# Optimization experiments

Hardware: AMD Instinct MI355X
Metric: run time of the kernel (lower is better)

## Reference

```python
import jax, jax.numpy as jnp
import numpy as np

TEMP = 0.07
HARD_K = 512
EMB_D = 768
PROJ_D = 128
QUEUE = 32768
BATCH = 2048
NUM_CLASSES = 2


def setup_inputs() -> dict:
    key = jax.random.key(0)
    ks = jax.random.split(key, 8)
    embeddings = jax.random.normal(ks[0], (BATCH, EMB_D), dtype=jnp.float32)
    labels = jax.random.randint(ks[1], (BATCH,), 0, NUM_CLASSES)
    # projector params: Linear(D,D) -> ReLU -> Linear(D,128)
    W1 = jax.random.normal(ks[2], (EMB_D, EMB_D), dtype=jnp.float32) * 0.02
    b1 = jnp.zeros((EMB_D,), dtype=jnp.float32)
    W2 = jax.random.normal(ks[3], (EMB_D, PROJ_D), dtype=jnp.float32) * 0.02
    b2 = jnp.zeros((PROJ_D,), dtype=jnp.float32)
    # queue buffers: L2-normalized random embeddings (as in __init__) with valid labels
    qe = jax.random.normal(ks[4], (QUEUE, PROJ_D), dtype=jnp.float32)
    queue_embeddings = qe / jnp.linalg.norm(qe, axis=1, keepdims=True)
    queue_labels = jax.random.randint(ks[5], (QUEUE,), 0, NUM_CLASSES)
    return {
        'embeddings': embeddings, 'labels': labels,
        'W1': W1, 'b1': b1, 'W2': W2, 'b2': b2,
        'queue_embeddings': queue_embeddings, 'queue_labels': queue_labels,
    }


def reference(embeddings, labels, W1, b1, W2, b2, queue_embeddings, queue_labels):
    n = embeddings.shape[0]
    # projector + L2 normalize
    h = jax.nn.relu(embeddings @ W1 + b1)
    z = h @ W2 + b2
    z = z / jnp.linalg.norm(z, axis=1, keepdims=True)  # (N, 128)

    # pairwise in-batch similarities, scaled by temperature
    S = (z @ z.T) / TEMP  # (N, N)
    same = labels[:, None] == labels[None, :]
    eye = jnp.eye(n, dtype=bool)
    pos_mask = same & ~eye           # positives: same label, not self
    neg_mask = ~same                 # in-batch negatives: different label

    # logsumexp over in-batch negatives per anchor (-inf rows -> -inf, handled by logaddexp)
    neg_batch = jnp.where(neg_mask, S, -jnp.inf)
    lse_batch = jax.scipy.special.logsumexp(neg_batch, axis=1)  # (N,)

    # hard negatives from queue: opposite-label, top-K by similarity
    sims_q = z @ queue_embeddings.T  # (N, Q)
    opp = (queue_labels[None, :] != labels[:, None]) & (queue_labels[None, :] >= 0)
    masked_q = jnp.where(opp, sims_q, -jnp.inf)
    topk_vals, _ = jax.lax.top_k(masked_q, HARD_K)  # (N, K); -inf pads drop from logsumexp
    # fallback (no opposite-label entries): first K queue embeddings regardless of label
    fallback = sims_q[:, :HARD_K]
    has_opp = opp.any(axis=1, keepdims=True)
    neg_q = jnp.where(has_opp, topk_vals, fallback) / TEMP
    lse_queue = jax.scipy.special.logsumexp(neg_q, axis=1)  # (N,)

    # all negatives for anchor i: batch negatives ++ queue hard negatives
    lse_neg = jnp.logaddexp(lse_batch, lse_queue)  # (N,)

    # per positive pair (i, j): log_prob = pos_sim - logsumexp([pos_sim, negs])
    log_prob = S - jnp.logaddexp(S, lse_neg[:, None])  # (N, N)
    losses = jnp.where(pos_mask, -log_prob, 0.0)
    count = pos_mask.sum()
    return jnp.where(count > 0, losses.sum() / count.astype(losses.dtype), 0.0)
```

## Files before the change

### kernel.cpp

```cpp
#include <hip/hip_runtime.h>
#include <hip/hip_fp16.h>

#define BATCH_N   2048
#define EMB_D_    768
#define PROJ_D_   128
#define QUEUE_N   32768
#define HARD_K_   512
static constexpr float INV_T  = 1.0f / 0.07f;
static constexpr float WLO    = 0.12f;
static constexpr float S8ENC  = 255.0f / 0.88f;
static constexpr float BINW   = 0.88f / 255.0f;

typedef __attribute__((ext_vector_type(8))) short short8;
typedef __attribute__((ext_vector_type(4))) short short4v;
typedef __attribute__((ext_vector_type(4))) float f32x4;

__device__ __forceinline__ unsigned short f2bf(float f) {
    unsigned u = __float_as_uint(f);
    unsigned r = u + 0x7fffu + ((u >> 16) & 1u);
    return (unsigned short)(r >> 16);
}
__device__ __forceinline__ float bf2f(short s) {
    return __uint_as_float(((unsigned)(unsigned short)s) << 16);
}
__device__ __forceinline__ int opp_of(int mylab, const int* __restrict__ qcnt) {
    const int same = (mylab == 0) ? qcnt[0] : ((mylab == 1) ? qcnt[1] : 0);
    return qcnt[2] - same;
}

__global__ void __launch_bounds__(256) mfma_s_pack(const short* __restrict__ Ab,
                                                   const short* __restrict__ Bb,
                                                   short* __restrict__ C, int N) {
    __shared__ __align__(16) short As[128 * 128];
    __shared__ __align__(16) short Bs[128 * 128];
    const int t = threadIdx.x;
    const int lane = t & 63, wv = t >> 6;
    const int l16 = lane & 15, l4 = lane >> 4;
    const int m0 = blockIdx.y * 128, n0 = blockIdx.x * 128;

    #pragma unroll
    for (int it = 0; it < 8; ++it) {
        const int r = it * 4 + wv, row = r * 4 + l4, cg = l16 ^ (row & 15);
        __builtin_amdgcn_global_load_lds(
            (const __attribute__((address_space(1))) void*)(Ab + (size_t)(m0 + row) * 128 + cg * 8),
            (__attribute__((address_space(3))) void*)(As + r * 512), 16, 0, 0);
    }
    #pragma unroll
    for (int it = 0; it < 8; ++it) {
        const int r = it * 4 + wv, row = r * 4 + l4, cg = l16 ^ (row & 15);
        __builtin_amdgcn_global_load_lds(
            (const __attribute__((address_space(1))) void*)(Bb + (size_t)(n0 + row) * 128 + cg * 8),
            (__attribute__((address_space(3))) void*)(Bs + r * 512), 16, 0, 0);
    }
    __syncthreads();

    const int wm = (wv & 1) * 64, wn = (wv >> 1) * 64;
    f32x4 acc[4][4];
    #pragma unroll
    for (int i = 0; i < 4; ++i)
        #pragma unroll
        for (int j = 0; j < 4; ++j) acc[i][j] = f32x4{0.f, 0.f, 0.f, 0.f};

    #pragma unroll
    for (int ks = 0; ks < 4; ++ks) {
        short8 af[4], bfr[4];
        const int ch = (ks * 4 + l4) ^ l16;
        #pragma unroll
        for (int i = 0; i < 4; ++i) {
            af[i]  = *(const short8*)(As + (wm + i * 16 + l16) * 128 + ch * 8);
            bfr[i] = *(const short8*)(Bs + (wn + i * 16 + l16) * 128 + ch * 8);
        }
        #pragma unroll
        for (int i = 0; i < 4; ++i)
            #pragma unroll
            for (int j = 0; j < 4; ++j)
                acc[i][j] = __builtin_amdgcn_mfma_f32_16x16x32_bf16(af[i], bfr[j], acc[i][j], 0, 0, 0);
    }
    #pragma unroll
    for (int i = 0; i < 4; ++i)
        #pragma unroll
        for (int r = 0; r < 4; ++r) {
            const int m = m0 + wm + i * 16 + l4 * 4 + r;
            union { unsigned short u[4]; uint2 d; } pk;
            #pragma unroll
            for (int j = 0; j < 4; ++j) pk.u[j] = f2bf(acc[i][j][r]);
            *(uint2*)(C + (size_t)m * N + n0 + wn + l16 * 4) = pk.d;
        }
}

__global__ void __launch_bounds__(256) mfma_mask8(const short* __restrict__ Ab,
                                                  const short* __restrict__ Bb,
                                                  unsigned char* __restrict__ codes,
                                                  const int* __restrict__ rlabp,
                                                  const int* __restrict__ qlabp,
                                                  const int* __restrict__ colidx,
                                                  const int* __restrict__ rowmap,
                                                  const int* __restrict__ qcnt,
                                                  const int* __restrict__ rcnt) {
    const int m0 = blockIdx.y * 128;
    const int c0 = qcnt[0], c1v = qcnt[1], r0 = rcnt[0];
    int lo, hi;
    if (m0 + 128 <= r0)      { lo = c0; hi = c0 + c1v; }
    else if (m0 >= r0)       { lo = 0;  hi = c0; }
    else                     { lo = 0;  hi = c0 + c1v; }
    const int bs = blockIdx.x * 512;
    if (bs + 512 <= lo || bs >= hi) return;

    __shared__ __align__(16) short As[128 * 128];
    __shared__ __align__(16) short Bs[128 * 128];
    const int t = threadIdx.x;
    const int lane = t & 63, wv = t >> 6;
    const int l16 = lane & 15, l4 = lane >> 4;
    const int wm = (wv & 1) * 64, wn = (wv >> 1) * 64;

    #pragma unroll
    for (int it = 0; it < 8; ++it) {
        const int r = it * 4 + wv, row = r * 4 + l4, cg = l16 ^ (row & 15);
        const int srow = rowmap[m0 + row];
        __builtin_amdgcn_global_load_lds(
            (const __attribute__((address_space(1))) void*)(Ab + (size_t)srow * 128 + cg * 8),
            (__attribute__((address_space(3))) void*)(As + r * 512), 16, 0, 0);
    }
    {
        const int n0 = bs;
        #pragma unroll
        for (int it = 0; it < 8; ++it) {
            const int r = it * 4 + wv, row = r * 4 + l4, cg = l16 ^ (row & 15);
            const int scol = colidx[n0 + row];
            __builtin_amdgcn_global_load_lds(
                (const __attribute__((address_space(1))) void*)(Bb + (size_t)scol * 128 + cg * 8),
                (__attribute__((address_space(3))) void*)(Bs + r * 512), 16, 0, 0);
        }
    }

    int la[16];
    #pragma unroll
    for (int i = 0; i < 4; ++i)
        #pragma unroll
        for (int r = 0; r < 4; ++r)
            la[i * 4 + r] = rlabp[m0 + wm + i * 16 + l4 * 4 + r];
    const float C0 = 1.0f - WLO * S8ENC;
    __syncthreads();

    #pragma unroll
    for (int tt = 0; tt < 4; ++tt) {
        const int n0 = bs + tt * 128;

        f32x4 acc[4][4];
        #pragma unroll
        for (int i = 0; i < 4; ++i)
            #pragma unroll
            for (int j = 0; j < 4; ++j) acc[i][j] = f32x4{0.f, 0.f, 0.f, 0.f};

        #pragma unroll
        for (int ks = 0; ks < 4; ++ks) {
            short8 af[4], bfr[4];
            const int ch = (ks * 4 + l4) ^ l16;
            #pragma unroll
            for (int i = 0; i < 4; ++i) {
                af[i]  = *(const short8*)(As + (wm + i * 16 + l16) * 128 + ch * 8);
                bfr[i] = *(const short8*)(Bs + (wn + i * 16 + l16) * 128 + ch * 8);
            }
            #pragma unroll
            for (int i = 0; i < 4; ++i)
                #pragma unroll
                for (int j = 0; j < 4; ++j)
                    acc[i][j] = __builtin_amdgcn_mfma_f32_16x16x32_bf16(af[i], bfr[j], acc[i][j], 0, 0, 0);
        }

        if (tt < 3) {
            __syncthreads();
            const int n1 = bs + (tt + 1) * 128;
            #pragma unroll
            for (int it = 0; it < 8; ++it) {
                const int r = it * 4 + wv, row = r * 4 + l4, cg = l16 ^ (row & 15);
                const int scol = colidx[n1 + row];
                __builtin_amdgcn_global_load_lds(
                    (const __attribute__((address_space(1))) void*)(Bb + (size_t)scol * 128 + cg * 8),
                    (__attribute__((address_space(3))) void*)(Bs + r * 512), 16, 0, 0);
            }
        }

        float a0[4], a1[4];
        #pragma unroll
        for (int j = 0; j < 4; ++j) {
            const int q = qlabp[n0 + wn + j * 16 + l16];
            a0[j] = (q >= 0 && q != 0) ? C0 : -1e9f;
            a1[j] = (q >= 0 && q != 1) ? C0 : -1e9f;
        }
        #pragma unroll
        for (int i = 0; i < 4; ++i) {
            #pragma unroll
            for (int r = 0; r < 4; ++r) {
                const int m  = m0 + wm + i * 16 + l4 * 4 + r;
                const bool z = (la[i * 4 + r] == 0);
                unsigned pk = 0;
                #pragma unroll
                for (int j = 0; j < 4; ++j) {
                    const float add = z ? a0[j] : a1[j];
                    const float f = fmaf(acc[i][j][r], S8ENC, add);
#if __has_builtin(__builtin_amdgcn_cvt_pk_u8_f32)
                    pk = __builtin_amdgcn_cvt_pk_u8_f32(f, j, pk);
#else
                    const unsigned c = (unsigned)fminf(fmaxf(f, 0.0f), 255.0f);
                    pk |= c << (8 * j);
#endif
                }
                *(unsigned*)(codes + (size_t)m * QUEUE_N + n0 + wn + l16 * 4) = pk;
            }
        }
        if (tt < 3) __syncthreads();
    }
}

__global__ void __launch_bounds__(256) mfma_h64(const short* __restrict__ Ab,
                                                const short* __restrict__ Bb,
                                                const float* __restrict__ bias,
                                                short* __restrict__ C,
                                                int N, int K) {
    __shared__ __align__(16) short As[64 * 128];
    __shared__ __align__(16) short Bs[128 * 128];
    const int t = threadIdx.x;
    const int lane = t & 63, wv = t >> 6;
    const int l16 = lane & 15, l4 = lane >> 4;
    const int m0 = blockIdx.y * 64, n0 = blockIdx.x * 128;
    const int wn = wv * 32;

    f32x4 acc[4][2];
    #pragma unroll
    for (int i = 0; i < 4; ++i)
        #pragma unroll
        for (int j = 0; j < 2; ++j) acc[i][j] = f32x4{0.f, 0.f, 0.f, 0.f};

    for (int kb = 0; kb < K; kb += 128) {
        __syncthreads();
        #pragma unroll
        for (int it = 0; it < 4; ++it) {
            const int r = it * 4 + wv, row = r * 4 + l4, cg = l16 ^ (row & 15);
            __builtin_amdgcn_global_load_lds(
                (const __attribute__((address_space(1))) void*)(Ab + (size_t)(m0 + row) * K + kb + cg * 8),
                (__attribute__((address_space(3))) void*)(As + r * 512), 16, 0, 0);
        }
        #pragma unroll
        for (int it = 0; it < 8; ++it) {
            const int r = it * 4 + wv, row = r * 4 + l4, cg = l16 ^ (row & 15);
            __builtin_amdgcn_global_load_lds(
                (const __attribute__((address_space(1))) void*)(Bb + (size_t)(n0 + row) * K + kb + cg * 8),
                (__attribute__((address_space(3))) void*)(Bs + r * 512), 16, 0, 0);
        }
        __syncthreads();
        #pragma unroll
        for (int ks = 0; ks < 4; ++ks) {
            short8 af[4], bfr[2];
            const int ch = (ks * 4 + l4) ^ l16;
            #pragma unroll
            for (int i = 0; i < 4; ++i)
                af[i] = *(const short8*)(As + (i * 16 + l16) * 128 + ch * 8);
            #pragma unroll
            for (int j = 0; j < 2; ++j)
                bfr[j] = *(const short8*)(Bs + (wn + j * 16 + l16) * 128 + ch * 8);
            #pragma unroll
            for (int i = 0; i < 4; ++i)
                #pragma unroll
                for (int j = 0; j < 2; ++j)
                    acc[i][j] = __builtin_amdgcn_mfma_f32_16x16x32_bf16(af[i], bfr[j], acc[i][j], 0, 0, 0);
        }
    }

    float bsv[2];
    #pragma unroll
    for (int j = 0; j < 2; ++j) bsv[j] = bias[n0 + wn + j * 16 + l16];
    #pragma unroll
    for (int i = 0; i < 4; ++i)
        #pragma unroll
        for (int r = 0; r < 4; ++r) {
            const int m = m0 + i * 16 + l4 * 4 + r;
            #pragma unroll
            for (int j = 0; j < 2; ++j) {
                const int n = n0 + wn + j * 16 + l16;
                const float v = fmaxf(acc[i][j][r] + bsv[j], 0.0f);
                C[(size_t)m * N + n] = (short)f2bf(v);
            }
        }
}

__global__ void __launch_bounds__(256) mfma_z_norm64(const short* __restrict__ Ab,
                                                     const short* __restrict__ Bb,
                                                     const float* __restrict__ bias,
                                                     short* __restrict__ zb) {
    __shared__ __align__(16) short As[64 * 128];
    __shared__ __align__(16) short Bs[128 * 128];
    __shared__ float ssq[64];
    const int t = threadIdx.x;
    const int lane = t & 63, wv = t >> 6;
    const int l16 = lane & 15, l4 = lane >> 4;
    const int m0 = blockIdx.x * 64;
    const int wn = wv * 32;
    const int K = EMB_D_;

    if (t < 64) ssq[t] = 0.0f;

    f32x4 acc[4][2];
    #pragma unroll
    for (int i = 0; i < 4; ++i)
        #pragma unroll
        for (int j = 0; j < 2; ++j) acc[i][j] = f32x4{0.f, 0.f, 0.f, 0.f};

    for (int kb = 0; kb < K; kb += 128) {
        __syncthreads();
        #pragma unroll
        for (int it = 0; it < 4; ++it) {
            const int r = it * 4 + wv, row = r * 4 + l4, cg = l16 ^ (row & 15);
            __builtin_amdgcn_global_load_lds(
                (const __attribute__((address_space(1))) void*)(Ab + (size_t)(m0 + row) * K + kb + cg * 8),
                (__attribute__((address_space(3))) void*)(As + r * 512), 16, 0, 0);
        }
        #pragma unroll
        for (int it = 0; it < 8; ++it) {
            const int r = it * 4 + wv, row = r * 4 + l4, cg = l16 ^ (row & 15);
            __builtin_amdgcn_global_load_lds(
                (const __attribute__((address_space(1))) void*)(Bb + (size_t)(row) * K + kb + cg * 8),
                (__attribute__((address_space(3))) void*)(Bs + r * 512), 16, 0, 0);
        }
        __syncthreads();
        #pragma unroll
        for (int ks = 0; ks < 4; ++ks) {
            short8 af[4], bfr[2];
            const int ch = (ks * 4 + l4) ^ l16;
            #pragma unroll
            for (int i = 0; i < 4; ++i)
                af[i] = *(const short8*)(As + (i * 16 + l16) * 128 + ch * 8);
            #pragma unroll
            for (int j = 0; j < 2; ++j)
                bfr[j] = *(const short8*)(Bs + (wn + j * 16 + l16) * 128 + ch * 8);
            #pragma unroll
            for (int i = 0; i < 4; ++i)
                #pragma unroll
                for (int j = 0; j < 2; ++j)
                    acc[i][j] = __builtin_amdgcn_mfma_f32_16x16x32_bf16(af[i], bfr[j], acc[i][j], 0, 0, 0);
        }
    }

    float bsv[2];
    #pragma unroll
    for (int j = 0; j < 2; ++j) bsv[j] = bias[wn + j * 16 + l16];
    #pragma unroll
    for (int i = 0; i < 4; ++i)
        #pragma unroll
        for (int r = 0; r < 4; ++r) {
            float p = 0.0f;
            #pragma unroll
            for (int j = 0; j < 2; ++j) {
                acc[i][j][r] += bsv[j];
                p += acc[i][j][r] * acc[i][j][r];
            }
            #pragma unroll
            for (int o = 8; o > 0; o >>= 1) p += __shfl_xor(p, o);
            if (l16 == 0) atomicAdd(&ssq[i * 16 + l4 * 4 + r], p);
        }
    __syncthreads();
    #pragma unroll
    for (int i = 0; i < 4; ++i)
        #pragma unroll
        for (int r = 0; r < 4; ++r) {
            const int lrow = i * 16 + l4 * 4 + r;
            const float inv = rsqrtf(ssq[lrow]);
            #pragma unroll
            for (int j = 0; j < 2; ++j)
                zb[(size_t)(m0 + lrow) * PROJ_D_ + wn + j * 16 + l16] =
                    (short)f2bf(acc[i][j][r] * inv);
        }
}

__global__ void __launch_bounds__(256) prep(const float* __restrict__ emb, short* __restrict__ embb,
                                            const float* __restrict__ queue, short* __restrict__ qb,
                                            const int* __restrict__ qlab, int* __restrict__ qcnt,
                                            const float* __restrict__ W1, short* __restrict__ w1t,
                                            const float* __restrict__ W2, short* __restrict__ w2t,
                                            const int* __restrict__ labels, int* __restrict__ rcnt) {
    __shared__ float tile[64][65];
    const int b = blockIdx.x, t = threadIdx.x;
    if (b < 1536) {
        const int i = b * 256 + t;
        const float4 f = ((const float4*)emb)[i];
        short4v o = {(short)f2bf(f.x), (short)f2bf(f.y), (short)f2bf(f.z), (short)f2bf(f.w)};
        ((short4v*)embb)[i] = o;
    } else if (b < 5632) {
        const int i = (b - 1536) * 256 + t;
        const float4 f = ((const float4*)queue)[i];
        short4v o = {(short)f2bf(f.x), (short)f2bf(f.y), (short)f2bf(f.z), (short)f2bf(f.w)};
        ((short4v*)qb)[i] = o;
    } else if (b < 5664) {
        const int i = (b - 5632) * 256 + t;
        int c0 = 0, c1 = 0, cv = 0;
        for (int j = i; j < QUEUE_N; j += 8192) {
            const int q = qlab[j];
            c0 += (q == 0); c1 += (q == 1); cv += (q >= 0);
        }
        #pragma unroll
        for (int o = 32; o > 0; o >>= 1) {
            c0 += __shfl_xor(c0, o); c1 += __shfl_xor(c1, o); cv += __shfl_xor(cv, o);
        }
        if ((t & 63) == 0) {
            atomicAdd(&qcnt[0], c0); atomicAdd(&qcnt[1], c1); atomicAdd(&qcnt[2], cv);
        }
    } else if (b < 5832) {
        const int bid = b - 5664;
        const float* A; short* At; int R, C, bx, by;
        if (bid < 144) { A = W1; At = w1t; R = EMB_D_; C = EMB_D_;  bx = (bid % 12) * 64; by = (bid / 12) * 64; }
        else { const int b2 = bid - 144; A = W2; At = w2t; R = EMB_D_; C = PROJ_D_; bx = (b2 & 1) * 64; by = (b2 >> 1) * 64; }
        const int tc = t & 63, tg = t >> 6;
        #pragma unroll
        for (int i = 0; i < 16; i++) {
            const int r = tg * 16 + i;
            tile[r][tc] = A[(size_t)(by + r) * C + bx + tc];
        }
        __syncthreads();
        #pragma unroll
        for (int i = 0; i < 16; i++) {
            const int r = tg * 16 + i;
            At[(size_t)(bx + r) * R + by + tc] = (short)f2bf(tile[tc][r]);
        }
    } else {
        int c = 0;
        for (int j = t; j < BATCH_N; j += 256) c += (labels[j] == 0);
        #pragma unroll
        for (int o = 32; o > 0; o >>= 1) c += __shfl_xor(c, o);
        if ((t & 63) == 0) atomicAdd(&rcnt[0], c);
    }
}

__global__ void __launch_bounds__(256) build_perm(const int* __restrict__ qlab,
                                                  const int* __restrict__ labels,
                                                  const int* __restrict__ qcnt,
                                                  const int* __restrict__ rcnt,
                                                  int* __restrict__ colidx,
                                                  int* __restrict__ qlabp,
                                                  int* __restrict__ rowmap,
                                                  int* __restrict__ rlabp,
                                                  int* __restrict__ pc) {
    const int t = threadIdx.x, lane = t & 63, wv = t >> 6;
    __shared__ int wcnt[4][3];
    __shared__ int gbase[3];
    const unsigned long long below = (1ull << lane) - 1ull;
    if (blockIdx.x < 128) {
        const int j = blockIdx.x * 256 + t;
        const int q = qlab[j];
        const int cls = (q == 0) ? 0 : ((q == 1) ? 1 : 2);
        const unsigned long long b0 = __ballot(cls == 0);
        const unsigned long long b1 = __ballot(cls == 1);
        const unsigned long long b2 = __ballot(cls == 2);
        const int rank = (cls == 0) ? __popcll(b0 & below)
                       : ((cls == 1) ? __popcll(b1 & below) : __popcll(b2 & below));
        if (lane == 0) {
            wcnt[wv][0] = __popcll(b0); wcnt[wv][1] = __popcll(b1); wcnt[wv][2] = __popcll(b2);
        }
        __syncthreads();
        if (t < 3) {
            const int tot = wcnt[0][t] + wcnt[1][t] + wcnt[2][t] + wcnt[3][t];
            gbase[t] = atomicAdd(&pc[t], tot);
        }
        __syncthreads();
        int wb = 0;
        #pragma unroll
        for (int w = 0; w < 4; ++w) if (w < wv) wb += wcnt[w][cls];
        const int cbase = (cls == 0) ? 0 : ((cls == 1) ? qcnt[0] : qcnt[0] + qcnt[1]);
        const int pos = cbase + gbase[cls] + wb + rank;
        colidx[pos] = j; qlabp[pos] = q;
    } else {
        const int r = (blockIdx.x - 128) * 256 + t;
        const int l = labels[r];
        const int cls = (l == 0) ? 0 : 1;
        const unsigned long long b0 = __ballot(cls == 0);
        const unsigned long long b1 = __ballot(cls == 1);
        const int rank = (cls == 0) ? __popcll(b0 & below) : __popcll(b1 & below);
        if (lane == 0) { wcnt[wv][0] = __popcll(b0); wcnt[wv][1] = __popcll(b1); }
        __syncthreads();
        if (t < 2) {
            const int tot = wcnt[0][t] + wcnt[1][t] + wcnt[2][t] + wcnt[3][t];
            gbase[t] = atomicAdd(&pc[3 + t], tot);
        }
        __syncthreads();
        int wb = 0;
        #pragma unroll
        for (int w = 0; w < 4; ++w) if (w < wv) wb += wcnt[w][cls];
        const int cbase = (cls == 0) ? 0 : rcnt[0];
        const int pos = cbase + gbase[cls] + wb + rank;
        rowmap[pos] = r; rlabp[pos] = l;
    }
}

__global__ void __launch_bounds__(256) topk_lse_u8(const unsigned char* __restrict__ codes,
                                                   const int* __restrict__ qcnt,
                                                   const int* __restrict__ rlabp,
                                                   const int* __restrict__ rowmap,
                                                   float* __restrict__ lseq,
                                                   int* __restrict__ flag) {
    const int p = blockIdx.x, t = threadIdx.x;
    const int orig  = rowmap[p];
    const int myLab = rlabp[p];
    const int opp   = opp_of(myLab, qcnt);
    if (opp < HARD_K_) {
        if (t == 0) flag[orig] = 0;
        return;
    }
    __shared__ int hist[256];
    __shared__ int suf[256];
    __shared__ int s_bin;
    __shared__ float scf[4];
    hist[t] = 0;
    __syncthreads();

    const int c0 = qcnt[0];
    const int lo = (myLab == 0) ? c0 : 0;
    const int hi = (myLab == 0) ? c0 + qcnt[1] : c0;
    const int klo = (lo & ~511) >> 4;
    const int khi = ((hi + 511) & ~511) >> 4;

    const uint4* rowp = (const uint4*)(codes + (size_t)p * QUEUE_N);
    for (int k = klo + t; k < khi; k += 256) {
        const uint4 u = rowp[k];
        const unsigned w[4] = {u.x, u.y, u.z, u.w};
        #pragma unroll
        for (int q = 0; q < 4; q++)
            #pragma unroll
            for (int s = 0; s < 4; s++) {
                const int c = (w[q] >> (8 * s)) & 0xFF;
                if (c) atomicAdd(&hist[c], 1);
            }
    }
    __syncthreads();

    suf[t] = hist[t];
    __syncthreads();
    for (int off = 1; off < 256; off <<= 1) {
        int add = (t + off < 256) ? suf[t + off] : 0;
        __syncthreads();
        suf[t] += add;
        __syncthreads();
    }
    const int total = suf[1];
    if (total < HARD_K_) {
        if (t == 0) flag[orig] = 0;
        return;
    }
    {
        const int above = (t < 255) ? suf[t + 1] : 0;
        if (suf[t] >= HARD_K_ && above < HARD_K_) s_bin = t;
    }
    __syncthreads();
    const int b = s_bin;

    float e = 0.0f;
    if (t > b && hist[t]) e = (float)hist[t] * __expf((WLO + ((float)t - 0.5f) * BINW - 1.0f) * INV_T);
    #pragma unroll
    for (int o = 32; o > 0; o >>= 1) e += __shfl_xor(e, o);
    if ((t & 63) == 0) scf[t >> 6] = e;
    __syncthreads();
    if (t == 0) {
        const float Eab  = scf[0] + scf[1] + scf[2] + scf[3];
        const int   cab  = (b < 255) ? suf[b + 1] : 0;
        const float ebin = __expf((WLO + ((float)b - 0.5f) * BINW - 1.0f) * INV_T);
        const float sadj = Eab + (float)(HARD_K_ - cab) * ebin;
        lseq[orig] = INV_T + __logf(sadj);
        flag[orig] = 1;
    }
}

__device__ __forceinline__ void find_crossing(int* hist, int* grp, int target,
                                              int* s_bin, int* s_chi) {
    const int t = threadIdx.x;
    const int b0 = hist[4*t], b1 = hist[4*t+1], b2 = hist[4*t+2], b3 = hist[4*t+3];
    grp[t] = b0 + b1 + b2 + b3;
    __syncthreads();
    for (int off = 1; off < 256; off <<= 1) {
        int add = (t + off < 256) ? grp[t + off] : 0;
        __syncthreads();
        grp[t] += add;
        __syncthreads();
    }
    int cab = (t < 255) ? grp[t + 1] : 0;
    const int hb[4] = {b0, b1, b2, b3};
    #pragma unroll
    for (int i = 3; i >= 0; i--) {
        const int h = hb[i];
        if (cab < target && cab + h >= target) { *s_bin = 4*t + i; *s_chi = cab; }
        cab += h;
    }
    __syncthreads();
}

#define FOR_ALL_VALS(BODY)                                                   \
    _Pragma("unroll")                                                        \
    for (int _k = 0; _k < 64; _k++) {                                        \
        const float2 _f = __half22float2(*(const __half2*)&dv[_k]);          \
        { const float v = _f.x; BODY }                                       \
        { const float v = _f.y; BODY }                                       \
    }

__global__ void __launch_bounds__(256) topk_lse_fallback(const short* __restrict__ zb,
                                                         const short* __restrict__ qb,
                                                         const int* __restrict__ labels,
                                                         const int* __restrict__ qlab,
                                                         const int* __restrict__ qcnt,
                                                         const int* __restrict__ flag,
                                                         float* __restrict__ lseq) {
    const int row = blockIdx.x, t = threadIdx.x;
    if (flag[row]) return;
    const int opp = opp_of(labels[row], qcnt);

    __shared__ float zrow[128];
    __shared__ int hist[1024];
    __shared__ int grp[256];
    __shared__ int s_bin, s_chi, s_bin2, s_chi2;
    __shared__ float scf[4]; __shared__ int sci[4];
    if (t < 128) zrow[t] = bf2f(zb[(size_t)row * 128 + t]);
    __syncthreads();

    const int mylab = labels[row];
    unsigned dv[64];
    float rm = -1e30f, rs = 0.0f;
    for (int k = 0; k < 128; k++) {
        const int j = t + 256 * k;
        float d = 0.0f;
        #pragma unroll
        for (int c = 0; c < 16; ++c) {
            const short8 qv = *(const short8*)(qb + (size_t)j * 128 + c * 8);
            #pragma unroll
            for (int e = 0; e < 8; ++e) d += zrow[c * 8 + e] * bf2f(qv[e]);
        }
        if (j < HARD_K_) {
            const float sv = d * INV_T;
            if (sv > rm) { rs = rs * __expf(rm - sv) + 1.0f; rm = sv; }
            else         { rs += __expf(sv - rm); }
        }
        const int q = qlab[j];
        const float mv = (q != mylab && q >= 0) ? d : -65504.0f;
        const __half h = __float2half(mv);
        unsigned short* p = (unsigned short*)&dv[k >> 1];
        p[k & 1] = *(const unsigned short*)&h;
    }

    if (opp == 0) {
        #pragma unroll
        for (int o = 32; o > 0; o >>= 1) {
            const float om = __shfl_xor(rm, o), os = __shfl_xor(rs, o);
            const float nm = fmaxf(rm, om);
            rs = rs * __expf(rm - nm) + os * __expf(om - nm);
            rm = nm;
        }
        if ((t & 63) == 0) { scf[t >> 6] = rm; ((float*)sci)[t >> 6] = rs; }
        __syncthreads();
        if (t == 0) {
            float M = -1e30f, Sx = 0.0f;
            for (int w = 0; w < 4; w++) {
                const float nm = fmaxf(M, scf[w]);
                Sx = Sx * __expf(M - nm) + ((float*)sci)[w] * __expf(scf[w] - nm);
                M = nm;
            }
            lseq[row] = M + __logf(Sx);
        }
        return;
    }
    if (opp < HARD_K_) {
        float mm = -1e30f, ss = 0.0f;
        FOR_ALL_VALS(
            if (v > -60000.0f) {
                const float sv = v * INV_T;
                if (sv > mm) { ss = ss * __expf(mm - sv) + 1.0f; mm = sv; }
                else         { ss += __expf(sv - mm); }
            } )
        #pragma unroll
        for (int o = 32; o > 0; o >>= 1) {
            const float om = __shfl_xor(mm, o), os = __shfl_xor(ss, o);
            const float nm = fmaxf(mm, om);
            ss = ss * __expf(mm - nm) + os * __expf(om - nm);
            mm = nm;
        }
        if ((t & 63) == 0) { scf[t >> 6] = mm; ((float*)sci)[t >> 6] = ss; }
        __syncthreads();
        if (t == 0) {
            float M = -1e30f, Sx = 0.0f;
            for (int w = 0; w < 4; w++) {
                const float nm = fmaxf(M, scf[w]);
                Sx = Sx * __expf(M - nm) + ((float*)sci)[w] * __expf(scf[w] - nm);
                M = nm;
            }
            lseq[row] = M + __logf(Sx);
        }
        return;
    }

    float mloc = -1e30f;
    FOR_ALL_VALS( mloc = fmaxf(mloc, v); )
    #pragma unroll
    for (int o = 32; o > 0; o >>= 1) mloc = fmaxf(mloc, __shfl_xor(mloc, o));
    if ((t & 63) == 0) scf[t >> 6] = mloc;
    __syncthreads();
    const float m = fmaxf(fmaxf(scf[0], scf[1]), fmaxf(scf[2], scf[3]));

    int c1 = 0, c2 = 0;
    const float w1 = m - 0.25f, w2 = m - 1.0f;
    FOR_ALL_VALS( c1 += (v >= w1); c2 += (v >= w2); )
    #pragma unroll
    for (int o = 32; o > 0; o >>= 1) { c1 += __shfl_xor(c1, o); c2 += __shfl_xor(c2, o); }
    if ((t & 63) == 0) { sci[t >> 6] = c1; }
    __syncthreads();
    const int C1 = sci[0] + sci[1] + sci[2] + sci[3];
    __syncthreads();
    if ((t & 63) == 0) { sci[t >> 6] = c2; }
    __syncthreads();
    const int C2 = sci[0] + sci[1] + sci[2] + sci[3];

    float lo;
    if      (C1 >= HARD_K_) lo = w1;
    else if (C2 >= HARD_K_) lo = w2;
    else                    lo = -1.01f;
    const float range = m - lo;
    const float scale = 1024.0f / range;

    for (int k = t; k < 1024; k += 256) hist[k] = 0;
    __syncthreads();
    FOR_ALL_VALS(
        if (v >= lo) {
            const float bf = fminf((v - lo) * scale, 1023.0f);
            atomicAdd(&hist[(int)bf], 1);
        } )
    __syncthreads();
    find_crossing(hist, grp, HARD_K_, &s_bin, &s_chi);
    const int   bin1 = s_bin, chi1 = s_chi;
    const float binw = range * (1.0f / 1024.0f);
    const float lo1  = lo + bin1 * binw;
    const float ssc  = 1024.0f / binw;

    for (int k = t; k < 1024; k += 256) hist[k] = 0;
    __syncthreads();
    FOR_ALL_VALS(
        if (v >= lo) {
            const float bf = fminf((v - lo) * scale, 1023.0f);
            if ((int)bf == bin1) {
                const float sf = fminf(fmaxf((v - lo1) * ssc, 0.0f), 1023.0f);
                atomicAdd(&hist[(int)sf], 1);
            }
        } )
    __syncthreads();
    find_crossing(hist, grp, HARD_K_ - chi1, &s_bin2, &s_chi2);
    const float thr = lo1 + s_bin2 * (binw * (1.0f / 1024.0f));

    float sl = 0.0f; int cg = 0;
    FOR_ALL_VALS( if (v > thr) { cg++; sl += __expf((v - m) * INV_T); } )
    #pragma unroll
    for (int o = 32; o > 0; o >>= 1) { sl += __shfl_xor(sl, o); cg += __shfl_xor(cg, o); }
    if ((t & 63) == 0) { scf[t >> 6] = sl; sci[t >> 6] = cg; }
    __syncthreads();
    if (t == 0) {
        const float slt = scf[0] + scf[1] + scf[2] + scf[3];
        const int   cgt = sci[0] + sci[1] + sci[2] + sci[3];
        const float sadj = slt + ((float)HARD_K_ - (float)cgt) * __expf((thr - m) * INV_T);
        lseq[row] = m * INV_T + __logf(sadj);
    }
}

__global__ void __launch_bounds__(256) batch_row_loss(const short* __restrict__ S,
                                                      const int* __restrict__ labels,
                                                      const float* __restrict__ lse_queue,
                                                      float* __restrict__ part_out,
                                                      int* __restrict__ cnt_out) {
    const int t = threadIdx.x;
    const int wv = t >> 6, lane = t & 63;
    const int row = blockIdx.x * 4 + wv;
    __shared__ int plab[BATCH_N];
    for (int idx = t; idx < BATCH_N; idx += 256) {
        const int col = (idx & ~63) + ((idx & 3) << 4) + ((idx >> 2) & 15);
        plab[idx] = labels[col];
    }
    __syncthreads();
    const int myLab = labels[row];
    const uint4* rp = (const uint4*)(S + (size_t)row * BATCH_N);

    float v[32]; int lb[32];
    #pragma unroll
    for (int kk = 0; kk < 4; kk++) {
        const uint4 u = rp[lane + 64 * kk];
        const unsigned w[4] = {u.x, u.y, u.z, u.w};
        const int base = (lane + 64 * kk) * 8;
        #pragma unroll
        for (int q = 0; q < 4; q++) {
            v[kk * 8 + 2 * q]     = __uint_as_float(w[q] << 16);
            v[kk * 8 + 2 * q + 1] = __uint_as_float(w[q] & 0xFFFF0000u);
            lb[kk * 8 + 2 * q]     = plab[base + 2 * q];
            lb[kk * 8 + 2 * q + 1] = plab[base + 2 * q + 1];
        }
    }

    const float REF = INV_T;
    float sneg = 0.0f;
    #pragma unroll
    for (int k = 0; k < 32; k++) {
        const float ev = __expf(v[k] * INV_T - REF);
        sneg += (lb[k] != myLab) ? ev : 0.0f;
    }
    #pragma unroll
    for (int o = 32; o > 0; o >>= 1) sneg += __shfl_xor(sneg, o);
    const float lseb = (sneg > 0.0f) ? REF + __logf(sneg) : -1e30f;
    const float Lq = lse_queue[row];
    const float mx0 = fmaxf(lseb, Lq), mn0 = fminf(lseb, Lq);
    const float L = mx0 + __logf(1.0f + __expf(mn0 - mx0));

    float part = 0.0f; int cnt = 0;
    #pragma unroll
    for (int k = 0; k < 32; k++) {
        const int idx = ((lane + 64 * (k >> 3)) * 8) + (k & 7);
        const int col = (idx & ~63) + ((idx & 3) << 4) + ((idx >> 2) & 15);
        if (lb[k] == myLab && col != row) {
            const float sv = v[k] * INV_T;
            const float mx = fmaxf(sv, L), mn = fminf(sv, L);
            part += (mx - sv) + __logf(1.0f + __expf(mn - mx));
            cnt++;
        }
    }
    #pragma unroll
    for (int o = 32; o > 0; o >>= 1) { part += __shfl_xor(part, o); cnt += __shfl_xor(cnt, o); }
    if (lane == 0) { part_out[row] = part; cnt_out[row] = cnt; }
}

__global__ void __launch_bounds__(256) finalize_loss(const float* __restrict__ part,
                                                     const int* __restrict__ cnt,
                                                     float* __restrict__ out) {
    const int t = threadIdx.x;
    float s = 0.0f; int c = 0;
    #pragma unroll
    for (int k = 0; k < 8; k++) { s += part[t + 256 * k]; c += cnt[t + 256 * k]; }
    #pragma unroll
    for (int o = 32; o > 0; o >>= 1) { s += __shfl_xor(s, o); c += __shfl_xor(c, o); }
    __shared__ float sf[4]; __shared__ int sc[4];
    if ((t & 63) == 0) { sf[t >> 6] = s; sc[t >> 6] = c; }
    __syncthreads();
    if (t == 0) {
        const float st = sf[0] + sf[1] + sf[2] + sf[3];
        const int   ct = sc[0] + sc[1] + sc[2] + sc[3];
        out[0] = (ct > 0) ? (st / (float)ct) : 0.0f;
    }
}

extern "C" void kernel_launch(void* const* d_in, const int* in_sizes, int n_in,
                              void* d_out, int out_size, void* d_ws, size_t ws_size,
                              hipStream_t stream) {
    const float* emb    = (const float*)d_in[0];
    const int*   labels = (const int*)  d_in[1];
    const float* W1     = (const float*)d_in[2];
    const float* b1     = (const float*)d_in[3];
    const float* W2     = (const float*)d_in[4];
    const float* b2     = (const float*)d_in[5];
    const float* queue  = (const float*)d_in[6];
    const int*   qlab   = (const int*)  d_in[7];

    char* ws = (char*)d_ws;
    short*         Sbuf  = (short*)        (ws);
    unsigned char* codes = (unsigned char*)(ws + 16777216);
    short*         embb  = (short*)        (ws + 83886080);
    short*         hbf   = (short*)        (ws + 87031808);
    short*         zb    = (short*)        (ws + 90177536);
    short*         qb    = (short*)        (ws + 90701824);
    short*         w1t   = (short*)        (ws + 99090432);
    short*         w2t   = (short*)        (ws + 100270080);
    float*         lseq  = (float*)        (ws + 100466688);
    int*           flag  = (int*)          (ws + 100474880);
    int*           qcnt  = (int*)          (ws + 100483072);
    float*         partb = (float*)        (ws + 100483136);
    int*           cntb  = (int*)          (ws + 100491328);
    int*           rcnt  = (int*)          (ws + 100499520);
    int*           pc    = (int*)          (ws + 100499584);
    int*           colidx= (int*)          (ws + 100499648);
    int*           qlabp = (int*)          (ws + 100630720);
    int*           rowmap= (int*)          (ws + 100761792);
    int*           rlabp = (int*)          (ws + 100769984);

    hipMemsetAsync(ws + 100474880, 0, 24768, stream);

    dim3 blk(256);
    prep<<<dim3(5833), blk, 0, stream>>>(emb, embb, queue, qb, qlab, qcnt, W1, w1t, W2, w2t, labels, rcnt);
    build_perm<<<dim3(136), blk, 0, stream>>>(qlab, labels, qcnt, rcnt, colidx, qlabp, rowmap, rlabp, pc);
    mfma_h64<<<dim3(EMB_D_ / 128, BATCH_N / 64), blk, 0, stream>>>(embb, w1t, b1, hbf, EMB_D_, EMB_D_);
    mfma_z_norm64<<<dim3(BATCH_N / 64), blk, 0, stream>>>(hbf, w2t, b2, zb);
    mfma_mask8<<<dim3(QUEUE_N / 512, BATCH_N / 128), blk, 0, stream>>>(zb, qb, codes, rlabp, qlabp, colidx, rowmap, qcnt, rcnt);
    topk_lse_u8<<<BATCH_N, blk, 0, stream>>>(codes, qcnt, rlabp, rowmap, lseq, flag);
    topk_lse_fallback<<<BATCH_N, blk, 0, stream>>>(zb, qb, labels, qlab, qcnt, flag, lseq);
    mfma_s_pack<<<dim3(BATCH_N / 128, BATCH_N / 128), blk, 0, stream>>>(zb, zb, Sbuf, BATCH_N);
    batch_row_loss<<<BATCH_N / 4, blk, 0, stream>>>(Sbuf, labels, lseq, partb, cntb);
    finalize_loss<<<1, blk, 0, stream>>>(partb, cntb, (float*)d_out);
}
```

Measured before the change: 166.4 us.

## Fuse launches: merge perm build into z-norm, and topk, fallback, S-GEMM into one kernel

Result: slower. 192.6 us (+15.7%).

```diff
diff --git a/kernel.cpp b/kernel.cpp
--- a/kernel.cpp
+++ b/kernel.cpp
@@ -28,356 +28,13 @@
     return qcnt[2] - same;
 }
 
-__global__ void __launch_bounds__(256) mfma_s_pack(const short* __restrict__ Ab,
-                                                   const short* __restrict__ Bb,
-                                                   short* __restrict__ C, int N) {
-    __shared__ __align__(16) short As[128 * 128];
-    __shared__ __align__(16) short Bs[128 * 128];
-    const int t = threadIdx.x;
-    const int lane = t & 63, wv = t >> 6;
-    const int l16 = lane & 15, l4 = lane >> 4;
-    const int m0 = blockIdx.y * 128, n0 = blockIdx.x * 128;
-
-    #pragma unroll
-    for (int it = 0; it < 8; ++it) {
-        const int r = it * 4 + wv, row = r * 4 + l4, cg = l16 ^ (row & 15);
-        __builtin_amdgcn_global_load_lds(
-            (const __attribute__((address_space(1))) void*)(Ab + (size_t)(m0 + row) * 128 + cg * 8),
-            (__attribute__((address_space(3))) void*)(As + r * 512), 16, 0, 0);
-    }
-    #pragma unroll
-    for (int it = 0; it < 8; ++it) {
-        const int r = it * 4 + wv, row = r * 4 + l4, cg = l16 ^ (row & 15);
-        __builtin_amdgcn_global_load_lds(
-            (const __attribute__((address_space(1))) void*)(Bb + (size_t)(n0 + row) * 128 + cg * 8),
-            (__attribute__((address_space(3))) void*)(Bs + r * 512), 16, 0, 0);
-    }
-    __syncthreads();
-
-    const int wm = (wv & 1) * 64, wn = (wv >> 1) * 64;
-    f32x4 acc[4][4];
-    #pragma unroll
-    for (int i = 0; i < 4; ++i)
-        #pragma unroll
-        for (int j = 0; j < 4; ++j) acc[i][j] = f32x4{0.f, 0.f, 0.f, 0.f};
-
-    #pragma unroll
-    for (int ks = 0; ks < 4; ++ks) {
-        short8 af[4], bfr[4];
-        const int ch = (ks * 4 + l4) ^ l16;
-        #pragma unroll
-        for (int i = 0; i < 4; ++i) {
-            af[i]  = *(const short8*)(As + (wm + i * 16 + l16) * 128 + ch * 8);
-            bfr[i] = *(const short8*)(Bs + (wn + i * 16 + l16) * 128 + ch * 8);
-        }
-        #pragma unroll
-        for (int i = 0; i < 4; ++i)
-            #pragma unroll
-            for (int j = 0; j < 4; ++j)
-                acc[i][j] = __builtin_amdgcn_mfma_f32_16x16x32_bf16(af[i], bfr[j], acc[i][j], 0, 0, 0);
-    }
-    #pragma unroll
-    for (int i = 0; i < 4; ++i)
-        #pragma unroll
-        for (int r = 0; r < 4; ++r) {
-            const int m = m0 + wm + i * 16 + l4 * 4 + r;
-            union { unsigned short u[4]; uint2 d; } pk;
-            #pragma unroll
-            for (int j = 0; j < 4; ++j) pk.u[j] = f2bf(acc[i][j][r]);
-            *(uint2*)(C + (size_t)m * N + n0 + wn + l16 * 4) = pk.d;
-        }
-}
-
-__global__ void __launch_bounds__(256) mfma_mask8(const short* __restrict__ Ab,
-                                                  const short* __restrict__ Bb,
-                                                  unsigned char* __restrict__ codes,
-                                                  const int* __restrict__ rlabp,
-                                                  const int* __restrict__ qlabp,
-                                                  const int* __restrict__ colidx,
-                                                  const int* __restrict__ rowmap,
-                                                  const int* __restrict__ qcnt,
-                                                  const int* __restrict__ rcnt) {
-    const int m0 = blockIdx.y * 128;
-    const int c0 = qcnt[0], c1v = qcnt[1], r0 = rcnt[0];
-    int lo, hi;
-    if (m0 + 128 <= r0)      { lo = c0; hi = c0 + c1v; }
-    else if (m0 >= r0)       { lo = 0;  hi = c0; }
-    else                     { lo = 0;  hi = c0 + c1v; }
-    const int bs = blockIdx.x * 512;
-    if (bs + 512 <= lo || bs >= hi) return;
-
-    __shared__ __align__(16) short As[128 * 128];
-    __shared__ __align__(16) short Bs[128 * 128];
-    const int t = threadIdx.x;
-    const int lane = t & 63, wv = t >> 6;
-    const int l16 = lane & 15, l4 = lane >> 4;
-    const int wm = (wv & 1) * 64, wn = (wv >> 1) * 64;
-
-    #pragma unroll
-    for (int it = 0; it < 8; ++it) {
-        const int r = it * 4 + wv, row = r * 4 + l4, cg = l16 ^ (row & 15);
-        const int srow = rowmap[m0 + row];
-        __builtin_amdgcn_global_load_lds(
-            (const __attribute__((address_space(1))) void*)(Ab + (size_t)srow * 128 + cg * 8),
-            (__attribute__((address_space(3))) void*)(As + r * 512), 16, 0, 0);
-    }
-    {
-        const int n0 = bs;
-        #pragma unroll
-        for (int it = 0; it < 8; ++it) {
-            const int r = it * 4 + wv, row = r * 4 + l4, cg = l16 ^ (row & 15);
-            const int scol = colidx[n0 + row];
-            __builtin_amdgcn_global_load_lds(
-                (const __attribute__((address_space(1))) void*)(Bb + (size_t)scol * 128 + cg * 8),
-                (__attribute__((address_space(3))) void*)(Bs + r * 512), 16, 0, 0);
-        }
-    }
-
-    int la[16];
-    #pragma unroll
-    for (int i = 0; i < 4; ++i)
-        #pragma unroll
-        for (int r = 0; r < 4; ++r)
-            la[i * 4 + r] = rlabp[m0 + wm + i * 16 + l4 * 4 + r];
-    const float C0 = 1.0f - WLO * S8ENC;
-    __syncthreads();
-
-    #pragma unroll
-    for (int tt = 0; tt < 4; ++tt) {
-        const int n0 = bs + tt * 128;
-
-        f32x4 acc[4][4];
-        #pragma unroll
-        for (int i = 0; i < 4; ++i)
-            #pragma unroll
-            for (int j = 0; j < 4; ++j) acc[i][j] = f32x4{0.f, 0.f, 0.f, 0.f};
-
-        #pragma unroll
-        for (int ks = 0; ks < 4; ++ks) {
-            short8 af[4], bfr[4];
-            const int ch = (ks * 4 + l4) ^ l16;
-            #pragma unroll
-            for (int i = 0; i < 4; ++i) {
-                af[i]  = *(const short8*)(As + (wm + i * 16 + l16) * 128 + ch * 8);
-                bfr[i] = *(const short8*)(Bs + (wn + i * 16 + l16) * 128 + ch * 8);
-            }
-            #pragma unroll
-            for (int i = 0; i < 4; ++i)
-                #pragma unroll
-                for (int j = 0; j < 4; ++j)
-                    acc[i][j] = __builtin_amdgcn_mfma_f32_16x16x32_bf16(af[i], bfr[j], acc[i][j], 0, 0, 0);
-        }
-
-        if (tt < 3) {
-            __syncthreads();
-            const int n1 = bs + (tt + 1) * 128;
-            #pragma unroll
-            for (int it = 0; it < 8; ++it) {
-                const int r = it * 4 + wv, row = r * 4 + l4, cg = l16 ^ (row & 15);
-                const int scol = colidx[n1 + row];
-                __builtin_amdgcn_global_load_lds(
-                    (const __attribute__((address_space(1))) void*)(Bb + (size_t)scol * 128 + cg * 8),
-                    (__attribute__((address_space(3))) void*)(Bs + r * 512), 16, 0, 0);
-            }
-        }
-
-        float a0[4], a1[4];
-        #pragma unroll
-        for (int j = 0; j < 4; ++j) {
-            const int q = qlabp[n0 + wn + j * 16 + l16];
-            a0[j] = (q >= 0 && q != 0) ? C0 : -1e9f;
-            a1[j] = (q >= 0 && q != 1) ? C0 : -1e9f;
-        }
-        #pragma unroll
-        for (int i = 0; i < 4; ++i) {
-            #pragma unroll
-            for (int r = 0; r < 4; ++r) {
-                const int m  = m0 + wm + i * 16 + l4 * 4 + r;
-                const bool z = (la[i * 4 + r] == 0);
-                unsigned pk = 0;
-                #pragma unroll
-                for (int j = 0; j < 4; ++j) {
-                    const float add = z ? a0[j] : a1[j];
-                    const float f = fmaf(acc[i][j][r], S8ENC, add);
-#if __has_builtin(__builtin_amdgcn_cvt_pk_u8_f32)
-                    pk = __builtin_amdgcn_cvt_pk_u8_f32(f, j, pk);
-#else
-                    const unsigned c = (unsigned)fminf(fmaxf(f, 0.0f), 255.0f);
-                    pk |= c << (8 * j);
-#endif
-                }
-                *(unsigned*)(codes + (size_t)m * QUEUE_N + n0 + wn + l16 * 4) = pk;
-            }
-        }
-        if (tt < 3) __syncthreads();
-    }
-}
-
-__global__ void __launch_bounds__(256) mfma_h64(const short* __restrict__ Ab,
-                                                const short* __restrict__ Bb,
-                                                const float* __restrict__ bias,
-                                                short* __restrict__ C,
-                                                int N, int K) {
-    __shared__ __align__(16) short As[64 * 128];
-    __shared__ __align__(16) short Bs[128 * 128];
-    const int t = threadIdx.x;
-    const int lane = t & 63, wv = t >> 6;
-    const int l16 = lane & 15, l4 = lane >> 4;
-    const int m0 = blockIdx.y * 64, n0 = blockIdx.x * 128;
-    const int wn = wv * 32;
-
-    f32x4 acc[4][2];
-    #pragma unroll
-    for (int i = 0; i < 4; ++i)
-        #pragma unroll
-        for (int j = 0; j < 2; ++j) acc[i][j] = f32x4{0.f, 0.f, 0.f, 0.f};
-
-    for (int kb = 0; kb < K; kb += 128) {
-        __syncthreads();
-        #pragma unroll
-        for (int it = 0; it < 4; ++it) {
-            const int r = it * 4 + wv, row = r * 4 + l4, cg = l16 ^ (row & 15);
-            __builtin_amdgcn_global_load_lds(
-                (const __attribute__((address_space(1))) void*)(Ab + (size_t)(m0 + row) * K + kb + cg * 8),
-                (__attribute__((address_space(3))) void*)(As + r * 512), 16, 0, 0);
-        }
-        #pragma unroll
-        for (int it = 0; it < 8; ++it) {
-            const int r = it * 4 + wv, row = r * 4 + l4, cg = l16 ^ (row & 15);
-            __builtin_amdgcn_global_load_lds(
-                (const __attribute__((address_space(1))) void*)(Bb + (size_t)(n0 + row) * K + kb + cg * 8),
-                (__attribute__((address_space(3))) void*)(Bs + r * 512), 16, 0, 0);
-        }
-        __syncthreads();
-        #pragma unroll
-        for (int ks = 0; ks < 4; ++ks) {
-            short8 af[4], bfr[2];
-            const int ch = (ks * 4 + l4) ^ l16;
-            #pragma unroll
-            for (int i = 0; i < 4; ++i)
-                af[i] = *(const short8*)(As + (i * 16 + l16) * 128 + ch * 8);
-            #pragma unroll
-            for (int j = 0; j < 2; ++j)
-                bfr[j] = *(const short8*)(Bs + (wn + j * 16 + l16) * 128 + ch * 8);
-            #pragma unroll
-            for (int i = 0; i < 4; ++i)
-                #pragma unroll
-                for (int j = 0; j < 2; ++j)
-                    acc[i][j] = __builtin_amdgcn_mfma_f32_16x16x32_bf16(af[i], bfr[j], acc[i][j], 0, 0, 0);
-        }
-    }
-
-    float bsv[2];
-    #pragma unroll
-    for (int j = 0; j < 2; ++j) bsv[j] = bias[n0 + wn + j * 16 + l16];
-    #pragma unroll
-    for (int i = 0; i < 4; ++i)
-        #pragma unroll
-        for (int r = 0; r < 4; ++r) {
-            const int m = m0 + i * 16 + l4 * 4 + r;
-            #pragma unroll
-            for (int j = 0; j < 2; ++j) {
-                const int n = n0 + wn + j * 16 + l16;
-                const float v = fmaxf(acc[i][j][r] + bsv[j], 0.0f);
-                C[(size_t)m * N + n] = (short)f2bf(v);
-            }
-        }
-}
-
-__global__ void __launch_bounds__(256) mfma_z_norm64(const short* __restrict__ Ab,
-                                                     const short* __restrict__ Bb,
-                                                     const float* __restrict__ bias,
-                                                     short* __restrict__ zb) {
-    __shared__ __align__(16) short As[64 * 128];
-    __shared__ __align__(16) short Bs[128 * 128];
-    __shared__ float ssq[64];
-    const int t = threadIdx.x;
-    const int lane = t & 63, wv = t >> 6;
-    const int l16 = lane & 15, l4 = lane >> 4;
-    const int m0 = blockIdx.x * 64;
-    const int wn = wv * 32;
-    const int K = EMB_D_;
-
-    if (t < 64) ssq[t] = 0.0f;
-
-    f32x4 acc[4][2];
-    #pragma unroll
-    for (int i = 0; i < 4; ++i)
-        #pragma unroll
-        for (int j = 0; j < 2; ++j) acc[i][j] = f32x4{0.f, 0.f, 0.f, 0.f};
-
-    for (int kb = 0; kb < K; kb += 128) {
-        __syncthreads();
-        #pragma unroll
-        for (int it = 0; it < 4; ++it) {
-            const int r = it * 4 + wv, row = r * 4 + l4, cg = l16 ^ (row & 15);
-            __builtin_amdgcn_global_load_lds(
-                (const __attribute__((address_space(1))) void*)(Ab + (size_t)(m0 + row) * K + kb + cg * 8),
-                (__attribute__((address_space(3))) void*)(As + r * 512), 16, 0, 0);
-        }
-        #pragma unroll
-        for (int it = 0; it < 8; ++it) {
-            const int r = it * 4 + wv, row = r * 4 + l4, cg = l16 ^ (row & 15);
-            __builtin_amdgcn_global_load_lds(
-                (const __attribute__((address_space(1))) void*)(Bb + (size_t)(row) * K + kb + cg * 8),
-                (__attribute__((address_space(3))) void*)(Bs + r * 512), 16, 0, 0);
-        }
-        __syncthreads();
-        #pragma unroll
-        for (int ks = 0; ks < 4; ++ks) {
-            short8 af[4], bfr[2];
-            const int ch = (ks * 4 + l4) ^ l16;
-            #pragma unroll
-            for (int i = 0; i < 4; ++i)
-                af[i] = *(const short8*)(As + (i * 16 + l16) * 128 + ch * 8);
-            #pragma unroll
-            for (int j = 0; j < 2; ++j)
-                bfr[j] = *(const short8*)(Bs + (wn + j * 16 + l16) * 128 + ch * 8);
-            #pragma unroll
-            for (int i = 0; i < 4; ++i)
-                #pragma unroll
-                for (int j = 0; j < 2; ++j)
-                    acc[i][j] = __builtin_amdgcn_mfma_f32_16x16x32_bf16(af[i], bfr[j], acc[i][j], 0, 0, 0);
-        }
-    }
-
-    float bsv[2];
-    #pragma unroll
-    for (int j = 0; j < 2; ++j) bsv[j] = bias[wn + j * 16 + l16];
-    #pragma unroll
-    for (int i = 0; i < 4; ++i)
-        #pragma unroll
-        for (int r = 0; r < 4; ++r) {
-            float p = 0.0f;
-            #pragma unroll
-            for (int j = 0; j < 2; ++j) {
-                acc[i][j][r] += bsv[j];
-                p += acc[i][j][r] * acc[i][j][r];
-            }
-            #pragma unroll
-            for (int o = 8; o > 0; o >>= 1) p += __shfl_xor(p, o);
-            if (l16 == 0) atomicAdd(&ssq[i * 16 + l4 * 4 + r], p);
-        }
-    __syncthreads();
-    #pragma unroll
-    for (int i = 0; i < 4; ++i)
-        #pragma unroll
-        for (int r = 0; r < 4; ++r) {
-            const int lrow = i * 16 + l4 * 4 + r;
-            const float inv = rsqrtf(ssq[lrow]);
-            #pragma unroll
-            for (int j = 0; j < 2; ++j)
-                zb[(size_t)(m0 + lrow) * PROJ_D_ + wn + j * 16 + l16] =
-                    (short)f2bf(acc[i][j][r] * inv);
-        }
-}
-
 __global__ void __launch_bounds__(256) prep(const float* __restrict__ emb, short* __restrict__ embb,
                                             const float* __restrict__ queue, short* __restrict__ qb,
-                                            const int* __restrict__ qlab, int* __restrict__ qcnt,
+                                            const int* __restrict__ qlab, int* __restrict__ qpart,
                                             const float* __restrict__ W1, short* __restrict__ w1t,
                                             const float* __restrict__ W2, short* __restrict__ w2t,
-                                            const int* __restrict__ labels, int* __restrict__ rcnt) {
+                                            const int* __restrict__ labels, int* __restrict__ rcnt,
+                                            int* __restrict__ pc) {
     __shared__ float tile[64][65];
     const int b = blockIdx.x, t = threadIdx.x;
     if (b < 1536) {
@@ -401,8 +58,15 @@
         for (int o = 32; o > 0; o >>= 1) {
             c0 += __shfl_xor(c0, o); c1 += __shfl_xor(c1, o); cv += __shfl_xor(cv, o);
         }
-        if ((t & 63) == 0) {
-            atomicAdd(&qcnt[0], c0); atomicAdd(&qcnt[1], c1); atomicAdd(&qcnt[2], cv);
+        int* red = (int*)tile;
+        const int wv = t >> 6;
+        if ((t & 63) == 0) { red[wv * 4 + 0] = c0; red[wv * 4 + 1] = c1; red[wv * 4 + 2] = cv; }
+        __syncthreads();
+        if (t == 0) {
+            const int bb = (b - 5632) * 4;
+            qpart[bb + 0] = red[0] + red[4] + red[8]  + red[12];
+            qpart[bb + 1] = red[1] + red[5] + red[9]  + red[13];
+            qpart[bb + 2] = red[2] + red[6] + red[10] + red[14];
         }
     } else if (b < 5832) {
         const int bid = b - 5664;
@@ -426,144 +90,371 @@
         for (int j = t; j < BATCH_N; j += 256) c += (labels[j] == 0);
         #pragma unroll
         for (int o = 32; o > 0; o >>= 1) c += __shfl_xor(c, o);
-        if ((t & 63) == 0) atomicAdd(&rcnt[0], c);
-    }
-}
-
-__global__ void __launch_bounds__(256) build_perm(const int* __restrict__ qlab,
+        int* red = (int*)tile;
+        if ((t & 63) == 0) red[t >> 6] = c;
+        __syncthreads();
+        if (t == 0) rcnt[0] = red[0] + red[1] + red[2] + red[3];
+        if (t < 8) pc[t] = 0;
+    }
+}
+
+__global__ void __launch_bounds__(256) mfma_h64(const short* __restrict__ Ab,
+                                                const short* __restrict__ Bb,
+                                                const float* __restrict__ bias,
+                                                short* __restrict__ C,
+                                                int N, int K) {
+    __shared__ __align__(16) short As[64 * 128];
+    __shared__ __align__(16) short Bs[128 * 128];
+    const int t = threadIdx.x;
+    const int lane = t & 63, wv = t >> 6;
+    const int l16 = lane & 15, l4 = lane >> 4;
+    const int m0 = blockIdx.y * 64, n0 = blockIdx.x * 128;
+    const int wn = wv * 32;
+
+    f32x4 acc[4][2];
+    #pragma unroll
+    for (int i = 0; i < 4; ++i)
+        #pragma unroll
+        for (int j = 0; j < 2; ++j) acc[i][j] = f32x4{0.f, 0.f, 0.f, 0.f};
+
+    for (int kb = 0; kb < K; kb += 128) {
+        __syncthreads();
+        #pragma unroll
+        for (int it = 0; it < 4; ++it) {
+            const int r = it * 4 + wv, row = r * 4 + l4, cg = l16 ^ (row & 15);
+            __builtin_amdgcn_global_load_lds(
+                (const __attribute__((address_space(1))) void*)(Ab + (size_t)(m0 + row) * K + kb + cg * 8),
+                (__attribute__((address_space(3))) void*)(As + r * 512), 16, 0, 0);
+        }
+        #pragma unroll
+        for (int it = 0; it < 8; ++it) {
+            const int r = it * 4 + wv, row = r * 4 + l4, cg = l16 ^ (row & 15);
+            __builtin_amdgcn_global_load_lds(
+                (const __attribute__((address_space(1))) void*)(Bb + (size_t)(n0 + row) * K + kb + cg * 8),
+                (__attribute__((address_space(3))) void*)(Bs + r * 512), 16, 0, 0);
+        }
+        __syncthreads();
+        #pragma unroll
+        for (int ks = 0; ks < 4; ++ks) {
+            short8 af[4], bfr[2];
+            const int ch = (ks * 4 + l4) ^ l16;
+            #pragma unroll
+            for (int i = 0; i < 4; ++i)
+                af[i] = *(const short8*)(As + (i * 16 + l16) * 128 + ch * 8);
+            #pragma unroll
+            for (int j = 0; j < 2; ++j)
+                bfr[j] = *(const short8*)(Bs + (wn + j * 16 + l16) * 128 + ch * 8);
+            #pragma unroll
+            for (int i = 0; i < 4; ++i)
+                #pragma unroll
+                for (int j = 0; j < 2; ++j)
+                    acc[i][j] = __builtin_amdgcn_mfma_f32_16x16x32_bf16(af[i], bfr[j], acc[i][j], 0, 0, 0);
+        }
+    }
+
+    float bsv[2];
+    #pragma unroll
+    for (int j = 0; j < 2; ++j) bsv[j] = bias[n0 + wn + j * 16 + l16];
+    #pragma unroll
+    for (int i = 0; i < 4; ++i)
+        #pragma unroll
+        for (int r = 0; r < 4; ++r) {
+            const int m = m0 + i * 16 + l4 * 4 + r;
+            #pragma unroll
+            for (int j = 0; j < 2; ++j) {
+                const int n = n0 + wn + j * 16 + l16;
+                const float v = fmaxf(acc[i][j][r] + bsv[j], 0.0f);
+                C[(size_t)m * N + n] = (short)f2bf(v);
+            }
+        }
+}
+
+__global__ void __launch_bounds__(256) znorm_perm(const short* __restrict__ Ab,
+                                                  const short* __restrict__ Bb,
+                                                  const float* __restrict__ bias,
+                                                  short* __restrict__ zb,
+                                                  const int* __restrict__ qlab,
                                                   const int* __restrict__ labels,
-                                                  const int* __restrict__ qcnt,
+                                                  const int* __restrict__ qpart,
                                                   const int* __restrict__ rcnt,
+                                                  int* __restrict__ qcnt,
                                                   int* __restrict__ colidx,
                                                   int* __restrict__ qlabp,
                                                   int* __restrict__ rowmap,
                                                   int* __restrict__ rlabp,
                                                   int* __restrict__ pc) {
-    const int t = threadIdx.x, lane = t & 63, wv = t >> 6;
+    __shared__ __align__(16) short As[32 * 128];
+    __shared__ __align__(16) short Bs[128 * 128];
+    __shared__ float ssq[32];
     __shared__ int wcnt[4][3];
     __shared__ int gbase[3];
-    const unsigned long long below = (1ull << lane) - 1ull;
-    if (blockIdx.x < 128) {
-        const int j = blockIdx.x * 256 + t;
-        const int q = qlab[j];
-        const int cls = (q == 0) ? 0 : ((q == 1) ? 1 : 2);
-        const unsigned long long b0 = __ballot(cls == 0);
-        const unsigned long long b1 = __ballot(cls == 1);
-        const unsigned long long b2 = __ballot(cls == 2);
-        const int rank = (cls == 0) ? __popcll(b0 & below)
-                       : ((cls == 1) ? __popcll(b1 & below) : __popcll(b2 & below));
-        if (lane == 0) {
-            wcnt[wv][0] = __popcll(b0); wcnt[wv][1] = __popcll(b1); wcnt[wv][2] = __popcll(b2);
-        }
-        __syncthreads();
-        if (t < 3) {
-            const int tot = wcnt[0][t] + wcnt[1][t] + wcnt[2][t] + wcnt[3][t];
-            gbase[t] = atomicAdd(&pc[t], tot);
-        }
-        __syncthreads();
-        int wb = 0;
-        #pragma unroll
-        for (int w = 0; w < 4; ++w) if (w < wv) wb += wcnt[w][cls];
-        const int cbase = (cls == 0) ? 0 : ((cls == 1) ? qcnt[0] : qcnt[0] + qcnt[1]);
-        const int pos = cbase + gbase[cls] + wb + rank;
-        colidx[pos] = j; qlabp[pos] = q;
-    } else {
-        const int r = (blockIdx.x - 128) * 256 + t;
-        const int l = labels[r];
-        const int cls = (l == 0) ? 0 : 1;
-        const unsigned long long b0 = __ballot(cls == 0);
-        const unsigned long long b1 = __ballot(cls == 1);
-        const int rank = (cls == 0) ? __popcll(b0 & below) : __popcll(b1 & below);
-        if (lane == 0) { wcnt[wv][0] = __popcll(b0); wcnt[wv][1] = __popcll(b1); }
-        __syncthreads();
-        if (t < 2) {
-            const int tot = wcnt[0][t] + wcnt[1][t] + wcnt[2][t] + wcnt[3][t];
-            gbase[t] = atomicAdd(&pc[3 + t], tot);
-        }
-        __syncthreads();
-        int wb = 0;
-        #pragma unroll
-        for (int w = 0; w < 4; ++w) if (w < wv) wb += wcnt[w][cls];
-        const int cbase = (cls == 0) ? 0 : rcnt[0];
-        const int pos = cbase + gbase[cls] + wb + rank;
-        rowmap[pos] = r; rlabp[pos] = l;
-    }
-}
-
-__global__ void __launch_bounds__(256) topk_lse_u8(const unsigned char* __restrict__ codes,
-                                                   const int* __restrict__ qcnt,
-                                                   const int* __restrict__ rlabp,
-                                                   const int* __restrict__ rowmap,
-                                                   float* __restrict__ lseq,
-                                                   int* __restrict__ flag) {
-    const int p = blockIdx.x, t = threadIdx.x;
-    const int orig  = rowmap[p];
-    const int myLab = rlabp[p];
-    const int opp   = opp_of(myLab, qcnt);
-    if (opp < HARD_K_) {
-        if (t == 0) flag[orig] = 0;
+    const int blk = blockIdx.x;
+    const int t = threadIdx.x;
+    const int lane = t & 63, wv = t >> 6;
+
+    if (blk >= 64) {
+        const unsigned long long below = (1ull << lane) - 1ull;
+        int q0 = 0, q1 = 0, qv = 0;
+        for (int i = 0; i < 32; ++i) {
+            q0 += qpart[i * 4]; q1 += qpart[i * 4 + 1]; qv += qpart[i * 4 + 2];
+        }
+        if (blk < 192) {
+            const int cb = blk - 64;
+            if (cb == 0 && t == 0) { qcnt[0] = q0; qcnt[1] = q1; qcnt[2] = qv; }
+            const int j = cb * 256 + t;
+            const int q = qlab[j];
+            const int cls = (q == 0) ? 0 : ((q == 1) ? 1 : 2);
+            const unsigned long long b0 = __ballot(cls == 0);
+            const unsigned long long b1 = __ballot(cls == 1);
+            const unsigned long long b2 = __ballot(cls == 2);
+            const int rank = (cls == 0) ? __popcll(b0 & below)
+                           : ((cls == 1) ? __popcll(b1 & below) : __popcll(b2 & below));
+            if (lane == 0) {
+                wcnt[wv][0] = __popcll(b0); wcnt[wv][1] = __popcll(b1); wcnt[wv][2] = __popcll(b2);
+            }
+            __syncthreads();
+            if (t < 3) {
+                const int tot = wcnt[0][t] + wcnt[1][t] + wcnt[2][t] + wcnt[3][t];
+                gbase[t] = atomicAdd(&pc[t], tot);
+            }
+            __syncthreads();
+            int wb = 0;
+            #pragma unroll
+            for (int w = 0; w < 4; ++w) if (w < wv) wb += wcnt[w][cls];
+            const int cbase = (cls == 0) ? 0 : ((cls == 1) ? q0 : q0 + q1);
+            const int pos = cbase + gbase[cls] + wb + rank;
+            colidx[pos] = j; qlabp[pos] = q;
+        } else {
+            const int r = (blk - 192) * 256 + t;
+            const int l = labels[r];
+            const int cls = (l == 0) ? 0 : 1;
+            const unsigned long long b0 = __ballot(cls == 0);
+            const unsigned long long b1 = __ballot(cls == 1);
+            const int rank = (cls == 0) ? __popcll(b0 & below) : __popcll(b1 & below);
+            if (lane == 0) { wcnt[wv][0] = __popcll(b0); wcnt[wv][1] = __popcll(b1); }
+            __syncthreads();
+            if (t < 2) {
+                const int tot = wcnt[0][t] + wcnt[1][t] + wcnt[2][t] + wcnt[3][t];
+                gbase[t] = atomicAdd(&pc[3 + t], tot);
+            }
+            __syncthreads();
+            int wb = 0;
+            #pragma unroll
+            for (int w = 0; w < 4; ++w) if (w < wv) wb += wcnt[w][cls];
+            const int cbase = (cls == 0) ? 0 : rcnt[0];
+            const int pos = cbase + gbase[cls] + wb + rank;
+            rowmap[pos] = r; rlabp[pos] = l;
+        }
         return;
     }
-    __shared__ int hist[256];
-    __shared__ int suf[256];
-    __shared__ int s_bin;
-    __shared__ float scf[4];
-    hist[t] = 0;
-    __syncthreads();
-
-    const int c0 = qcnt[0];
-    const int lo = (myLab == 0) ? c0 : 0;
-    const int hi = (myLab == 0) ? c0 + qcnt[1] : c0;
-    const int klo = (lo & ~511) >> 4;
-    const int khi = ((hi + 511) & ~511) >> 4;
-
-    const uint4* rowp = (const uint4*)(codes + (size_t)p * QUEUE_N);
-    for (int k = klo + t; k < khi; k += 256) {
-        const uint4 u = rowp[k];
-        const unsigned w[4] = {u.x, u.y, u.z, u.w};
-        #pragma unroll
-        for (int q = 0; q < 4; q++)
-            #pragma unroll
-            for (int s = 0; s < 4; s++) {
-                const int c = (w[q] >> (8 * s)) & 0xFF;
-                if (c) atomicAdd(&hist[c], 1);
-            }
-    }
-    __syncthreads();
-
-    suf[t] = hist[t];
-    __syncthreads();
-    for (int off = 1; off < 256; off <<= 1) {
-        int add = (t + off < 256) ? suf[t + off] : 0;
-        __syncthreads();
-        suf[t] += add;
-        __syncthreads();
-    }
-    const int total = suf[1];
-    if (total < HARD_K_) {
-        if (t == 0) flag[orig] = 0;
-        return;
-    }
-    {
-        const int above = (t < 255) ? suf[t + 1] : 0;
-        if (suf[t] >= HARD_K_ && above < HARD_K_) s_bin = t;
-    }
-    __syncthreads();
-    const int b = s_bin;
-
-    float e = 0.0f;
-    if (t > b && hist[t]) e = (float)hist[t] * __expf((WLO + ((float)t - 0.5f) * BINW - 1.0f) * INV_T);
-    #pragma unroll
-    for (int o = 32; o > 0; o >>= 1) e += __shfl_xor(e, o);
-    if ((t & 63) == 0) scf[t >> 6] = e;
-    __syncthreads();
-    if (t == 0) {
-        const float Eab  = scf[0] + scf[1] + scf[2] + scf[3];
-        const int   cab  = (b < 255) ? suf[b + 1] : 0;
-        const float ebin = __expf((WLO + ((float)b - 0.5f) * BINW - 1.0f) * INV_T);
-        const float sadj = Eab + (float)(HARD_K_ - cab) * ebin;
-        lseq[orig] = INV_T + __logf(sadj);
-        flag[orig] = 1;
+
+    const int l16 = lane & 15, l4 = lane >> 4;
+    const int m0 = blk * 32;
+    const int wn = wv * 32;
+    const int K = EMB_D_;
+
+    if (t < 32) ssq[t] = 0.0f;
+
+    f32x4 acc[2][2];
+    #pragma unroll
+    for (int i = 0; i < 2; ++i)
+        #pragma unroll
+        for (int j = 0; j < 2; ++j) acc[i][j] = f32x4{0.f, 0.f, 0.f, 0.f};
+
+    for (int kb = 0; kb < K; kb += 128) {
+        __syncthreads();
+        #pragma unroll
+        for (int it = 0; it < 2; ++it) {
+            const int r = it * 4 + wv, row = r * 4 + l4, cg = l16 ^ (row & 15);
+            __builtin_amdgcn_global_load_lds(
+                (const __attribute__((address_space(1))) void*)(Ab + (size_t)(m0 + row) * K + kb + cg * 8),
+                (__attribute__((address_space(3))) void*)(As + r * 512), 16, 0, 0);
+        }
+        #pragma unroll
+        for (int it = 0; it < 8; ++it) {
+            const int r = it * 4 + wv, row = r * 4 + l4, cg = l16 ^ (row & 15);
+            __builtin_amdgcn_global_load_lds(
+                (const __attribute__((address_space(1))) void*)(Bb + (size_t)(row) * K + kb + cg * 8),
+                (__attribute__((address_space(3))) void*)(Bs + r * 512), 16, 0, 0);
+        }
+        __syncthreads();
+        #pragma unroll
+        for (int ks = 0; ks < 4; ++ks) {
+            short8 af[2], bfr[2];
+            const int ch = (ks * 4 + l4) ^ l16;
+            #pragma unroll
+            for (int i = 0; i < 2; ++i)
+                af[i] = *(const short8*)(As + (i * 16 + l16) * 128 + ch * 8);
+            #pragma unroll
+            for (int j = 0; j < 2; ++j)
+                bfr[j] = *(const short8*)(Bs + (wn + j * 16 + l16) * 128 + ch * 8);
+            #pragma unroll
+            for (int i = 0; i < 2; ++i)
+                #pragma unroll
+                for (int j = 0; j < 2; ++j)
+                    acc[i][j] = __builtin_amdgcn_mfma_f32_16x16x32_bf16(af[i], bfr[j], acc[i][j], 0, 0, 0);
+        }
+    }
+
+    float bsv[2];
+    #pragma unroll
+    for (int j = 0; j < 2; ++j) bsv[j] = bias[wn + j * 16 + l16];
+    #pragma unroll
+    for (int i = 0; i < 2; ++i)
+        #pragma unroll
+        for (int r = 0; r < 4; ++r) {
+            float p = 0.0f;
+            #pragma unroll
+            for (int j = 0; j < 2; ++j) {
+                acc[i][j][r] += bsv[j];
+                p += acc[i][j][r] * acc[i][j][r];
+            }
+            #pragma unroll
+            for (int o = 8; o > 0; o >>= 1) p += __shfl_xor(p, o);
+            if (l16 == 0) atomicAdd(&ssq[i * 16 + l4 * 4 + r], p);
+        }
+    __syncthreads();
+    #pragma unroll
+    for (int i = 0; i < 2; ++i)
+        #pragma unroll
+        for (int r = 0; r < 4; ++r) {
+            const int lrow = i * 16 + l4 * 4 + r;
+            const float inv = rsqrtf(ssq[lrow]);
+            #pragma unroll
+            for (int j = 0; j < 2; ++j)
+                zb[(size_t)(m0 + lrow) * PROJ_D_ + wn + j * 16 + l16] =
+                    (short)f2bf(acc[i][j][r] * inv);
+        }
+}
+
+__global__ void __launch_bounds__(256) mfma_mask8(const short* __restrict__ Ab,
+                                                  const short* __restrict__ Bb,
+                                                  unsigned char* __restrict__ codes,
+                                                  const int* __restrict__ rlabp,
+                                                  const int* __restrict__ qlabp,
+                                                  const int* __restrict__ colidx,
+                                                  const int* __restrict__ rowmap,
+                                                  const int* __restrict__ qcnt,
+                                                  const int* __restrict__ rcnt) {
+    const int m0 = blockIdx.y * 128;
+    const int c0 = qcnt[0], c1v = qcnt[1], r0 = rcnt[0];
+    int lo, hi;
+    if (m0 + 128 <= r0)      { lo = c0; hi = c0 + c1v; }
+    else if (m0 >= r0)       { lo = 0;  hi = c0; }
+    else                     { lo = 0;  hi = c0 + c1v; }
+    const int bs = blockIdx.x * 512;
+    if (bs + 512 <= lo || bs >= hi) return;
+
+    __shared__ __align__(16) short As[128 * 128];
+    __shared__ __align__(16) short Bs[128 * 128];
+    const int t = threadIdx.x;
+    const int lane = t & 63, wv = t >> 6;
+    const int l16 = lane & 15, l4 = lane >> 4;
+    const int wm = (wv & 1) * 64, wn = (wv >> 1) * 64;
+
+    int ra[8], ca[32], la[16], qa[16];
+    #pragma unroll
+    for (int it = 0; it < 8; ++it)
+        ra[it] = rowmap[m0 + (it * 4 + wv) * 4 + l4];
+    #pragma unroll
+    for (int tt = 0; tt < 4; ++tt)
+        #pragma unroll
+        for (int it = 0; it < 8; ++it)
+            ca[tt * 8 + it] = colidx[bs + tt * 128 + (it * 4 + wv) * 4 + l4];
+    #pragma unroll
+    for (int i = 0; i < 4; ++i)
+        #pragma unroll
+        for (int r = 0; r < 4; ++r)
+            la[i * 4 + r] = rlabp[m0 + wm + i * 16 + l4 * 4 + r];
+    #pragma unroll
+    for (int tt = 0; tt < 4; ++tt)
+        #pragma unroll
+        for (int j = 0; j < 4; ++j)
+            qa[tt * 4 + j] = qlabp[bs + tt * 128 + wn + j * 16 + l16];
+
+    #pragma unroll
+    for (int it = 0; it < 8; ++it) {
+        const int r = it * 4 + wv, row = r * 4 + l4, cg = l16 ^ (row & 15);
+        __builtin_amdgcn_global_load_lds(
+            (const __attribute__((address_space(1))) void*)(Ab + (size_t)ra[it] * 128 + cg * 8),
+            (__attribute__((address_space(3))) void*)(As + r * 512), 16, 0, 0);
+    }
+    #pragma unroll
+    for (int it = 0; it < 8; ++it) {
+        const int r = it * 4 + wv, row = r * 4 + l4, cg = l16 ^ (row & 15);
+        __builtin_amdgcn_global_load_lds(
+            (const __attribute__((address_space(1))) void*)(Bb + (size_t)ca[it] * 128 + cg * 8),
+            (__attribute__((address_space(3))) void*)(Bs + r * 512), 16, 0, 0);
+    }
+    const float C0 = 1.0f - WLO * S8ENC;
+    __syncthreads();
+
+    #pragma unroll
+    for (int tt = 0; tt < 4; ++tt) {
+        const int n0 = bs + tt * 128;
+
+        f32x4 acc[4][4];
+        #pragma unroll
+        for (int i = 0; i < 4; ++i)
+            #pragma unroll
+            for (int j = 0; j < 4; ++j) acc[i][j] = f32x4{0.f, 0.f, 0.f, 0.f};
+
+        #pragma unroll
+        for (int ks = 0; ks < 4; ++ks) {
+            short8 af[4], bfr[4];
+            const int ch = (ks * 4 + l4) ^ l16;
+            #pragma unroll
+            for (int i = 0; i < 4; ++i) {
+                af[i]  = *(const short8*)(As + (wm + i * 16 + l16) * 128 + ch * 8);
+                bfr[i] = *(const short8*)(Bs + (wn + i * 16 + l16) * 128 + ch * 8);
+            }
+            #pragma unroll
+            for (int i = 0; i < 4; ++i)
+                #pragma unroll
+                for (int j = 0; j < 4; ++j)
+                    acc[i][j] = __builtin_amdgcn_mfma_f32_16x16x32_bf16(af[i], bfr[j], acc[i][j], 0, 0, 0);
+        }
+
+        if (tt < 3) {
+            __syncthreads();
+            #pragma unroll
+            for (int it = 0; it < 8; ++it) {
+                const int r = it * 4 + wv, row = r * 4 + l4, cg = l16 ^ (row & 15);
+                __builtin_amdgcn_global_load_lds(
+                    (const __attribute__((address_space(1))) void*)(Bb + (size_t)ca[(tt + 1) * 8 + it] * 128 + cg * 8),
+                    (__attribute__((address_space(3))) void*)(Bs + r * 512), 16, 0, 0);
+            }
+        }
+
+        float a0[4], a1[4];
+        #pragma unroll
+        for (int j = 0; j < 4; ++j) {
+            const int q = qa[tt * 4 + j];
+            a0[j] = (q >= 0 && q != 0) ? C0 : -1e9f;
+            a1[j] = (q >= 0 && q != 1) ? C0 : -1e9f;
+        }
+        #pragma unroll
+        for (int i = 0; i < 4; ++i) {
+            #pragma unroll
+            for (int r = 0; r < 4; ++r) {
+                const int m  = m0 + wm + i * 16 + l4 * 4 + r;
+                const bool z = (la[i * 4 + r] == 0);
+                unsigned pk = 0;
+                #pragma unroll
+                for (int j = 0; j < 4; ++j) {
+                    const float add = z ? a0[j] : a1[j];
+                    const float f = fmaf(acc[i][j][r], S8ENC, add);
+#if __has_builtin(__builtin_amdgcn_cvt_pk_u8_f32)
+                    pk = __builtin_amdgcn_cvt_pk_u8_f32(f, j, pk);
+#else
+                    const unsigned c = (unsigned)fminf(fmaxf(f, 0.0f), 255.0f);
+                    pk |= c << (8 * j);
+#endif
+                }
+                *(unsigned*)(codes + (size_t)m * QUEUE_N + n0 + wn + l16 * 4) = pk;
+            }
+        }
+        if (tt < 3) __syncthreads();
     }
 }
 
@@ -598,26 +489,152 @@
         { const float v = _f.y; BODY }                                       \
     }
 
-__global__ void __launch_bounds__(256) topk_lse_fallback(const short* __restrict__ zb,
-                                                         const short* __restrict__ qb,
-                                                         const int* __restrict__ labels,
-                                                         const int* __restrict__ qlab,
-                                                         const int* __restrict__ qcnt,
-                                                         const int* __restrict__ flag,
-                                                         float* __restrict__ lseq) {
-    const int row = blockIdx.x, t = threadIdx.x;
-    if (flag[row]) return;
-    const int opp = opp_of(labels[row], qcnt);
-
-    __shared__ float zrow[128];
-    __shared__ int hist[1024];
-    __shared__ int grp[256];
+__global__ void __launch_bounds__(256) tail_fused(const unsigned char* __restrict__ codes,
+                                                  const int* __restrict__ qcnt,
+                                                  const int* __restrict__ rlabp,
+                                                  const int* __restrict__ rowmap,
+                                                  const short* __restrict__ zb,
+                                                  const short* __restrict__ qb,
+                                                  const int* __restrict__ qlab,
+                                                  float* __restrict__ lseq,
+                                                  short* __restrict__ Sbuf) {
+    __shared__ __align__(16) short As[128 * 128];
+    __shared__ __align__(16) short Bs[128 * 128];
     __shared__ int s_bin, s_chi, s_bin2, s_chi2;
-    __shared__ float scf[4]; __shared__ int sci[4];
-    if (t < 128) zrow[t] = bf2f(zb[(size_t)row * 128 + t]);
-    __syncthreads();
-
-    const int mylab = labels[row];
+    __shared__ float scf[4];
+    __shared__ int sci[4];
+    const int bid = blockIdx.x, t = threadIdx.x;
+
+    if (bid >= BATCH_N) {
+        const int q = bid - BATCH_N;
+        const int lane = t & 63, wv = t >> 6;
+        const int l16 = lane & 15, l4 = lane >> 4;
+        const int m0 = (q >> 4) * 128, n0 = (q & 15) * 128;
+
+        #pragma unroll
+        for (int it = 0; it < 8; ++it) {
+            const int r = it * 4 + wv, row = r * 4 + l4, cg = l16 ^ (row & 15);
+            __builtin_amdgcn_global_load_lds(
+                (const __attribute__((address_space(1))) void*)(zb + (size_t)(m0 + row) * 128 + cg * 8),
+                (__attribute__((address_space(3))) void*)(As + r * 512), 16, 0, 0);
+        }
+        #pragma unroll
+        for (int it = 0; it < 8; ++it) {
+            const int r = it * 4 + wv, row = r * 4 + l4, cg = l16 ^ (row & 15);
+            __builtin_amdgcn_global_load_lds(
+                (const __attribute__((address_space(1))) void*)(zb + (size_t)(n0 + row) * 128 + cg * 8),
+                (__attribute__((address_space(3))) void*)(Bs + r * 512), 16, 0, 0);
+        }
+        __syncthreads();
+
+        const int wm = (wv & 1) * 64, wn = (wv >> 1) * 64;
+        f32x4 acc[4][4];
+        #pragma unroll
+        for (int i = 0; i < 4; ++i)
+            #pragma unroll
+            for (int j = 0; j < 4; ++j) acc[i][j] = f32x4{0.f, 0.f, 0.f, 0.f};
+
+        #pragma unroll
+        for (int ks = 0; ks < 4; ++ks) {
+            short8 af[4], bfr[4];
+            const int ch = (ks * 4 + l4) ^ l16;
+            #pragma unroll
+            for (int i = 0; i < 4; ++i) {
+                af[i]  = *(const short8*)(As + (wm + i * 16 + l16) * 128 + ch * 8);
+                bfr[i] = *(const short8*)(Bs + (wn + i * 16 + l16) * 128 + ch * 8);
+            }
+            #pragma unroll
+            for (int i = 0; i < 4; ++i)
+                #pragma unroll
+                for (int j = 0; j < 4; ++j)
+                    acc[i][j] = __builtin_amdgcn_mfma_f32_16x16x32_bf16(af[i], bfr[j], acc[i][j], 0, 0, 0);
+        }
+        #pragma unroll
+        for (int i = 0; i < 4; ++i)
+            #pragma unroll
+            for (int r = 0; r < 4; ++r) {
+                const int m = m0 + wm + i * 16 + l4 * 4 + r;
+                union { unsigned short u[4]; uint2 d; } pk;
+                #pragma unroll
+                for (int j = 0; j < 4; ++j) pk.u[j] = f2bf(acc[i][j][r]);
+                *(uint2*)(Sbuf + (size_t)m * BATCH_N + n0 + wn + l16 * 4) = pk.d;
+            }
+        return;
+    }
+
+    const int p = bid;
+    const int orig  = rowmap[p];
+    const int myLab = rlabp[p];
+    const int opp   = opp_of(myLab, qcnt);
+    bool fb = (opp < HARD_K_);
+    if (!fb) {
+        int* hist = (int*)Bs;
+        int* suf  = (int*)(Bs + 512);
+        hist[t] = 0;
+        __syncthreads();
+
+        const int c0 = qcnt[0];
+        const int lo = (myLab == 0) ? c0 : 0;
+        const int hi = (myLab == 0) ? c0 + qcnt[1] : c0;
+        const int klo = (lo & ~511) >> 4;
+        const int khi = ((hi + 511) & ~511) >> 4;
+
+        const uint4* rowp = (const uint4*)(codes + (size_t)p * QUEUE_N);
+        for (int k = klo + t; k < khi; k += 256) {
+            const uint4 u = rowp[k];
+            const unsigned w[4] = {u.x, u.y, u.z, u.w};
+            #pragma unroll
+            for (int q = 0; q < 4; q++)
+                #pragma unroll
+                for (int s = 0; s < 4; s++) {
+                    const int c = (w[q] >> (8 * s)) & 0xFF;
+                    if (c) atomicAdd(&hist[c], 1);
+                }
+        }
+        __syncthreads();
+
+        suf[t] = hist[t];
+        __syncthreads();
+        for (int off = 1; off < 256; off <<= 1) {
+            int add = (t + off < 256) ? suf[t + off] : 0;
+            __syncthreads();
+            suf[t] += add;
+            __syncthreads();
+        }
+        const int total = suf[1];
+        if (total >= HARD_K_) {
+            {
+                const int above = (t < 255) ? suf[t + 1] : 0;
+                if (suf[t] >= HARD_K_ && above < HARD_K_) s_bin = t;
+            }
+            __syncthreads();
+            const int b = s_bin;
+
+            float e = 0.0f;
+            if (t > b && hist[t]) e = (float)hist[t] * __expf((WLO + ((float)t - 0.5f) * BINW - 1.0f) * INV_T);
+            #pragma unroll
+            for (int o = 32; o > 0; o >>= 1) e += __shfl_xor(e, o);
+            if ((t & 63) == 0) scf[t >> 6] = e;
+            __syncthreads();
+            if (t == 0) {
+                const float Eab  = scf[0] + scf[1] + scf[2] + scf[3];
+                const int   cab  = (b < 255) ? suf[b + 1] : 0;
+                const float ebin = __expf((WLO + ((float)b - 0.5f) * BINW - 1.0f) * INV_T);
+                const float sadj = Eab + (float)(HARD_K_ - cab) * ebin;
+                lseq[orig] = INV_T + __logf(sadj);
+            }
+            return;
+        }
+        __syncthreads();
+    }
+
+    float* zrow = (float*)As;
+    int*   fh   = (int*)(As + 512);
+    int*   grp  = (int*)(As + 2560);
+    if (t < 128) zrow[t] = bf2f(zb[(size_t)orig * 128 + t]);
+    __syncthreads();
+
+    const int mylab = myLab;
     unsigned dv[64];
     float rm = -1e30f, rs = 0.0f;
     for (int k = 0; k < 128; k++) {
@@ -637,8 +654,8 @@
         const int q = qlab[j];
         const float mv = (q != mylab && q >= 0) ? d : -65504.0f;
         const __half h = __float2half(mv);
-        unsigned short* p = (unsigned short*)&dv[k >> 1];
-        p[k & 1] = *(const unsigned short*)&h;
+        unsigned short* pp = (unsigned short*)&dv[k >> 1];
+        pp[k & 1] = *(const unsigned short*)&h;
     }
 
     if (opp == 0) {
@@ -658,7 +675,7 @@
                 Sx = Sx * __expf(M - nm) + ((float*)sci)[w] * __expf(scf[w] - nm);
                 M = nm;
             }
-            lseq[row] = M + __logf(Sx);
+            lseq[orig] = M + __logf(Sx);
         }
         return;
     }
@@ -686,7 +703,7 @@
                 Sx = Sx * __expf(M - nm) + ((float*)sci)[w] * __expf(scf[w] - nm);
                 M = nm;
             }
-            lseq[row] = M + __logf(Sx);
+            lseq[orig] = M + __logf(Sx);
         }
         return;
     }
@@ -719,32 +736,32 @@
     const float range = m - lo;
     const float scale = 1024.0f / range;
 
-    for (int k = t; k < 1024; k += 256) hist[k] = 0;
+    for (int k = t; k < 1024; k += 256) fh[k] = 0;
     __syncthreads();
     FOR_ALL_VALS(
         if (v >= lo) {
             const float bf = fminf((v - lo) * scale, 1023.0f);
-            atomicAdd(&hist[(int)bf], 1);
+            atomicAdd(&fh[(int)bf], 1);
         } )
     __syncthreads();
-    find_crossing(hist, grp, HARD_K_, &s_bin, &s_chi);
+    find_crossing(fh, grp, HARD_K_, &s_bin, &s_chi);
     const int   bin1 = s_bin, chi1 = s_chi;
     const float binw = range * (1.0f / 1024.0f);
     const float lo1  = lo + bin1 * binw;
     const float ssc  = 1024.0f / binw;
 
-    for (int k = t; k < 1024; k += 256) hist[k] = 0;
+    for (int k = t; k < 1024; k += 256) fh[k] = 0;
     __syncthreads();
     FOR_ALL_VALS(
         if (v >= lo) {
             const float bf = fminf((v - lo) * scale, 1023.0f);
             if ((int)bf == bin1) {
                 const float sf = fminf(fmaxf((v - lo1) * ssc, 0.0f), 1023.0f);
-                atomicAdd(&hist[(int)sf], 1);
+                atomicAdd(&fh[(int)sf], 1);
             }
         } )
     __syncthreads();
-    find_crossing(hist, grp, HARD_K_ - chi1, &s_bin2, &s_chi2);
+    find_crossing(fh, grp, HARD_K_ - chi1, &s_bin2, &s_chi2);
     const float thr = lo1 + s_bin2 * (binw * (1.0f / 1024.0f));
 
     float sl = 0.0f; int cg = 0;
@@ -757,7 +774,7 @@
         const float slt = scf[0] + scf[1] + scf[2] + scf[3];
         const int   cgt = sci[0] + sci[1] + sci[2] + sci[3];
         const float sadj = slt + ((float)HARD_K_ - (float)cgt) * __expf((thr - m) * INV_T);
-        lseq[row] = m * INV_T + __logf(sadj);
+        lseq[orig] = m * INV_T + __logf(sadj);
     }
 }
 
@@ -865,28 +882,24 @@
     short*         w1t   = (short*)        (ws + 99090432);
     short*         w2t   = (short*)        (ws + 100270080);
     float*         lseq  = (float*)        (ws + 100466688);
-    int*           flag  = (int*)          (ws + 100474880);
-    int*           qcnt  = (int*)          (ws + 100483072);
-    float*         partb = (float*)        (ws + 100483136);
-    int*           cntb  = (int*)          (ws + 100491328);
-    int*           rcnt  = (int*)          (ws + 100499520);
-    int*           pc    = (int*)          (ws + 100499584);
-    int*           colidx= (int*)          (ws + 100499648);
-    int*           qlabp = (int*)          (ws + 100630720);
-    int*           rowmap= (int*)          (ws + 100761792);
-    int*           rlabp = (int*)          (ws + 100769984);
-
-    hipMemsetAsync(ws + 100474880, 0, 24768, stream);
+    int*           qcnt  = (int*)          (ws + 100474880);
+    int*           rcnt  = (int*)          (ws + 100474944);
+    int*           pc    = (int*)          (ws + 100475008);
+    int*           qpart = (int*)          (ws + 100475072);
+    float*         partb = (float*)        (ws + 100475584);
+    int*           cntb  = (int*)          (ws + 100483776);
+    int*           colidx= (int*)          (ws + 100491968);
+    int*           qlabp = (int*)          (ws + 100623040);
+    int*           rowmap= (int*)          (ws + 100754112);
+    int*           rlabp = (int*)          (ws + 100762304);
 
     dim3 blk(256);
-    prep<<<dim3(5833), blk, 0, stream>>>(emb, embb, queue, qb, qlab, qcnt, W1, w1t, W2, w2t, labels, rcnt);
-    build_perm<<<dim3(136), blk, 0, stream>>>(qlab, labels, qcnt, rcnt, colidx, qlabp, rowmap, rlabp, pc);
+    prep<<<dim3(5833), blk, 0, stream>>>(emb, embb, queue, qb, qlab, qpart, W1, w1t, W2, w2t, labels, rcnt, pc);
     mfma_h64<<<dim3(EMB_D_ / 128, BATCH_N / 64), blk, 0, stream>>>(embb, w1t, b1, hbf, EMB_D_, EMB_D_);
-    mfma_z_norm64<<<dim3(BATCH_N / 64), blk, 0, stream>>>(hbf, w2t, b2, zb);
+    znorm_perm<<<dim3(200), blk, 0, stream>>>(hbf, w2t, b2, zb, qlab, labels, qpart, rcnt,
+                                              qcnt, colidx, qlabp, rowmap, rlabp, pc);
     mfma_mask8<<<dim3(QUEUE_N / 512, BATCH_N / 128), blk, 0, stream>>>(zb, qb, codes, rlabp, qlabp, colidx, rowmap, qcnt, rcnt);
-    topk_lse_u8<<<BATCH_N, blk, 0, stream>>>(codes, qcnt, rlabp, rowmap, lseq, flag);
-    topk_lse_fallback<<<BATCH_N, blk, 0, stream>>>(zb, qb, labels, qlab, qcnt, flag, lseq);
-    mfma_s_pack<<<dim3(BATCH_N / 128, BATCH_N / 128), blk, 0, stream>>>(zb, zb, Sbuf, BATCH_N);
-    batch_row_loss<<<BATCH_N / 4, blk, 0, stream>>>(Sbuf, labels, lseq, partb, cntb);
+    tail_fused<<<dim3(BATCH_N + 256), blk, 0, stream>>>(codes, qcnt, rlabp, rowmap, zb, qb, qlab, lseq, Sbuf);
+    batch_row_loss<<<dim3(BATCH_N / 4), blk, 0, stream>>>(Sbuf, labels, lseq, partb, cntb);
     finalize_loss<<<1, blk, 0, stream>>>(partb, cntb, (float*)d_out);
 }
```
